# Performance work log

Hardware: AMD Instinct MI355X
Metric: run time of the kernel (lower is better)

The kernel has to match this reference:

```python
import jax, jax.numpy as jnp
import numpy as np

C0, C1, ED, H, L, K = 128, 32, 64, 4, 2, 16
RADIUS = 16.0
EPS = 1e-6


def _ln(x, g, b):
    m = jnp.mean(x, -1, keepdims=True)
    v = jnp.var(x, -1, keepdims=True)
    return (x - m) * jax.lax.rsqrt(v + 1e-5) * g + b


def _gather_nodes(x, idx):
    # x [B,N,...], idx [B,N,K] -> [B,N,K,...]
    return jax.vmap(lambda xb, ib: xb[ib])(x, idx)


def _gather_pairs(e, idx):
    # e [B,N,N,ED], idx [B,N,K] -> [B,N,K,ED]  (batched_index_select on dim=2)
    return jax.vmap(lambda eb, ib: jnp.take_along_axis(eb, ib[..., None], axis=1))(e, idx)


def _fiber_norm(f0, f1, g0, b0, g1, b1):
    # deg-0: LayerNorm + gelu; deg-1: phase-preserving norm on channel magnitudes
    f0n = jax.nn.gelu(_ln(f0, g0, b0))
    n1 = jnp.linalg.norm(f1, axis=-1)                       # [B,N,C1]
    f1n = f1 / (n1 + EPS)[..., None] * jax.nn.gelu(_ln(n1, g1, b1))[..., None]
    return f0n, f1n


def _tfn_kv(f0j, f1j, y1, r, WA, WB):
    # Equivariant TFN edge kernel: paths 0->0(l=0), 1->0(l=1), 0->1(l=1),
    # 1->1(l=0), 1->1(l=1, cross), 1->1(l=2, traceless Y2) with radial gates r.
    r1, r2, r3, r4, r5, r6 = jnp.split(
        r, [C0, C0 + C1, 2 * C0 + C1, 2 * C0 + 2 * C1, 2 * C0 + 3 * C1], axis=-1)
    dot1 = jnp.einsum('bnkcm,bnkm->bnkc', f1j, y1)          # [B,N,K,C1]
    in0 = jnp.concatenate([r1 * f0j, r2 * dot1], -1)        # [B,N,K,C0+C1]
    k0 = jnp.einsum('oc,bnkc->bnko', WA, in0)               # [B,N,K,C0]
    p3 = (r3 * f0j)[..., None] * y1[..., None, :]           # [B,N,K,C0,3]
    p4 = r4[..., None] * f1j
    p5 = r5[..., None] * jnp.cross(f1j, y1[..., None, :])
    p6 = r6[..., None] * (y1[..., None, :] * dot1[..., None] - f1j / 3.0)
    in1 = jnp.concatenate([p3, p4, p5, p6], axis=-2)        # [B,N,K,C0+3*C1,3]
    k1 = jnp.einsum('oc,bnkcm->bnkom', WB, in1)             # [B,N,K,C1,3]
    return k0, k1


def reference(node_feats, pair_feats, coords, eln_g, eln_b, Wi0, Wi1,
              ln0_g, ln0_b, n1_g, n1_b, Wq0, Wq1, WrK, WrV, WkA, WkB, WvA, WvB,
              Wb, Wo0, Wo1, alpha_attn, lnf0_g, lnf0_b, nf1_g, nf1_b,
              Wf0a, Wf0b, Wf1a, Wf1b, alpha_ff, Wp0, Wp1):
    B, N = node_feats.shape[:2]
    Na, CA, Cc, Oo = [coords[..., i, :] for i in range(4)]          # each [B,N,3]
    f1_in = jnp.stack([Na, Cc, Oo], axis=-2) - CA[..., None, :]     # [B,N,3,3]
    # kNN graph on CA coords (exclude self), radius mask at 16A
    d2 = jnp.sum((CA[:, :, None] - CA[:, None, :]) ** 2, -1)        # [B,N,N]
    d2 = d2 + jnp.eye(N, dtype=d2.dtype) * 1e9
    nv, idx = jax.lax.top_k(-d2, K)                                 # idx [B,N,K]
    dist = jnp.sqrt(jnp.maximum(-nv, 0.0))
    mask = dist <= RADIUS
    rel_pos = _gather_nodes(CA, idx) - CA[:, :, None]               # [B,N,K,3]
    rel_b = jax.lax.stop_gradient(rel_pos)                          # basis on detached rel_pos
    y1 = rel_b / (jnp.linalg.norm(rel_b, axis=-1, keepdims=True) + EPS)
    edges = _ln(_gather_pairs(pair_feats, idx), eln_g, eln_b)       # [B,N,K,ED]
    # project in
    f0 = jnp.einsum('oc,bnc->bno', Wi0, node_feats)                 # [B,N,C0]
    f1 = jnp.einsum('oc,bncm->bnom', Wi1, f1_in)                    # [B,N,C1,3]
    dh0, dh1 = C0 // H, C1 // H
    scale = 1.0 / np.sqrt(dh0 + 3 * dh1)
    for l in range(L):
        # ---- attention block (prenorm -> TFN attention -> rezero residual)
        x0, x1 = _fiber_norm(f0, f1, ln0_g[l], ln0_b[l], n1_g[l], n1_b[l])
        q0 = jnp.einsum('oc,bnc->bno', Wq0[l], x0)
        q1 = jnp.einsum('oc,bncm->bnom', Wq1[l], x1)
        x0j = _gather_nodes(x0, idx)                                # [B,N,K,C0]
        x1j = _gather_nodes(x1, idx)                                # [B,N,K,C1,3]
        rk = jnp.einsum('re,bnke->bnkr', WrK[l], edges)
        rv = jnp.einsum('re,bnke->bnkr', WrV[l], edges)
        k0, k1 = _tfn_kv(x0j, x1j, y1, rk, WkA[l], WkB[l])
        v0, v1 = _tfn_kv(x0j, x1j, y1, rv, WvA[l], WvB[l])
        q0h = q0.reshape(B, N, H, dh0)
        q1h = q1.reshape(B, N, H, dh1, 3)
        k0h = k0.reshape(B, N, K, H, dh0)
        k1h = k1.reshape(B, N, K, H, dh1, 3)
        v0h = v0.reshape(B, N, K, H, dh0)
        v1h = v1.reshape(B, N, K, H, dh1, 3)
        logits = (jnp.einsum('bnhc,bnkhc->bnhk', q0h, k0h)
                  + jnp.einsum('bnhcm,bnkhcm->bnhk', q1h, k1h)) * scale
        logits = logits + jnp.einsum('he,bnke->bnhk', Wb[l], edges)
        logits = jnp.where(mask[:, :, None, :], logits, -1e9)
        attn = jax.nn.softmax(logits, axis=-1)
        o0 = jnp.einsum('bnhk,bnkhc->bnhc', attn, v0h).reshape(B, N, C0)
        o1 = jnp.einsum('bnhk,bnkhcm->bnhcm', attn, v1h).reshape(B, N, C1, 3)
        f0 = f0 + alpha_attn[l] * jnp.einsum('oc,bnc->bno', Wo0[l], o0)
        f1 = f1 + alpha_attn[l] * jnp.einsum('oc,bncm->bnom', Wo1[l], o1)
        # ---- fiber feedforward (prenorm -> FF -> rezero residual)
        x0, x1 = _fiber_norm(f0, f1, lnf0_g[l], lnf0_b[l], nf1_g[l], nf1_b[l])
        h0 = jnp.einsum('oh,bnh->bno', Wf0b[l],
                        jax.nn.gelu(jnp.einsum('hc,bnc->bnh', Wf0a[l], x0)))
        h1 = jnp.einsum('hc,bncm->bnhm', Wf1a[l], x1)
        nh = jnp.linalg.norm(h1, axis=-1)
        h1 = h1 * (jax.nn.gelu(nh) / (nh + EPS))[..., None]
        h1 = jnp.einsum('oh,bnhm->bnom', Wf1b[l], h1)
        f0 = f0 + alpha_ff[l] * h0
        f1 = f1 + alpha_ff[l] * h1
    # project out + _to_output
    node_out = jnp.einsum('oc,bnc->bno', Wp0, f0)                   # [B,N,128]
    coords_out = CA[:, :, None, :] + jnp.einsum('oc,bncm->bnom', Wp1, f1)  # [B,N,3,3]
    return node_out, coords_out


def setup_inputs() -> dict:
    key = jax.random.key(0)
    ks = iter(jax.random.split(key, 64))
    def rn(shape, scale=1.0):
        return (jax.random.normal(next(ks), shape) * scale).astype(jnp.float32)
    B, N = 1, 1024
    RC = 2 * C0 + 4 * C1
    ca = jnp.cumsum(rn((B, N, 3), 1.5), axis=1)          # protein-like chain
    coords = ca[:, :, None, :] + rn((B, N, 4, 3), 0.5)
    inp = dict(
        node_feats=rn((B, N, 128)),
        pair_feats=rn((B, N, N, ED)),
        coords=coords,
        eln_g=jnp.ones((ED,), jnp.float32), eln_b=jnp.zeros((ED,), jnp.float32),
        Wi0=rn((C0, 128), 128 ** -0.5), Wi1=rn((C1, 3), 3 ** -0.5),
        ln0_g=jnp.ones((L, C0), jnp.float32), ln0_b=jnp.zeros((L, C0), jnp.float32),
        n1_g=jnp.ones((L, C1), jnp.float32), n1_b=jnp.zeros((L, C1), jnp.float32),
        Wq0=rn((L, C0, C0), C0 ** -0.5), Wq1=rn((L, C1, C1), C1 ** -0.5),
        WrK=rn((L, RC, ED), ED ** -0.5), WrV=rn((L, RC, ED), ED ** -0.5),
        WkA=rn((L, C0, C0 + C1), (C0 + C1) ** -0.5),
        WkB=rn((L, C1, C0 + 3 * C1), (C0 + 3 * C1) ** -0.5),
        WvA=rn((L, C0, C0 + C1), (C0 + C1) ** -0.5),
        WvB=rn((L, C1, C0 + 3 * C1), (C0 + 3 * C1) ** -0.5),
        Wb=rn((L, H, ED), ED ** -0.5),
        Wo0=rn((L, C0, C0), C0 ** -0.5), Wo1=rn((L, C1, C1), C1 ** -0.5),
        alpha_attn=jnp.full((L,), 0.5, jnp.float32),
        lnf0_g=jnp.ones((L, C0), jnp.float32), lnf0_b=jnp.zeros((L, C0), jnp.float32),
        nf1_g=jnp.ones((L, C1), jnp.float32), nf1_b=jnp.zeros((L, C1), jnp.float32),
        Wf0a=rn((L, 4 * C0, C0), C0 ** -0.5), Wf0b=rn((L, C0, 4 * C0), (4 * C0) ** -0.5),
        Wf1a=rn((L, 4 * C1, C1), C1 ** -0.5), Wf1b=rn((L, C1, 4 * C1), (4 * C1) ** -0.5),
        alpha_ff=jnp.full((L,), 0.5, jnp.float32),
        Wp0=rn((128, C0), C0 ** -0.5), Wp1=rn((3, C1), C1 ** -0.5),
    )
    return inp
```

## Files before the change

kernel.cpp:

```cpp
#include <hip/hip_runtime.h>
#include <hip/hip_bf16.h>
#include <math.h>

static constexpr int NN  = 1024;
static constexpr int KK  = 16;
static constexpr int C0c = 128;
static constexpr int C1c = 32;
static constexpr int EDc = 64;
static constexpr int Lc  = 2;
static constexpr int ENUM = NN * KK;
static constexpr int PL   = NN * C1c;
static constexpr int X1HS = NN * 32;
#define SCALE_ATTN 0.13363062095621219f

typedef __attribute__((ext_vector_type(8))) short s8v;
typedef __attribute__((ext_vector_type(4))) float f4v;

__device__ __forceinline__ float wsum64(float v) {
    for (int o = 32; o > 0; o >>= 1) v += __shfl_xor(v, o);
    return v;
}
__device__ __forceinline__ float gsum16(float v) {
    for (int o = 8; o > 0; o >>= 1) v += __shfl_xor(v, o, 16);
    return v;
}
__device__ __forceinline__ float gmax16(float v) {
    for (int o = 8; o > 0; o >>= 1) v = fmaxf(v, __shfl_xor(v, o, 16));
    return v;
}
__device__ __forceinline__ float gelu_f(float x) {
    float x3 = x * x * x;
    return 0.5f * x * (1.0f + tanhf(0.7978845608028654f * (x + 0.044715f * x3)));
}
__device__ __forceinline__ unsigned short f2bf(float x) {
    union { float f; unsigned int u; } v; v.f = x;
    unsigned int r = v.u + 0x7fffu + ((v.u >> 16) & 1u);
    return (unsigned short)(r >> 16);
}
__device__ __forceinline__ float bf2f(unsigned short u) {
    union { float f; unsigned int i; } v; v.i = ((unsigned int)u) << 16;
    return v.f;
}
__device__ __forceinline__ s8v ld8(const unsigned short* p) { return *(const s8v*)p; }
__device__ __forceinline__ f4v mfma16(s8v a, s8v b, f4v c) {
    return __builtin_amdgcn_mfma_f32_16x16x32_bf16(a, b, c, 0, 0, 0);
}

struct CvJob { const float* s; unsigned short* d; int n; };
struct CvJobs { CvJob j[20]; int n; int total; };

__global__ __launch_bounds__(256) void setup_kernel(CvJobs cj, int cvb,
                                                    const float* __restrict__ coords,
                                                    int* __restrict__ idx,
                                                    float* __restrict__ maskf,
                                                    float* __restrict__ y1,
                                                    const float* __restrict__ Wi1,
                                                    float* __restrict__ f1p) {
    __shared__ float ca[NN * 3];
    const int tid = threadIdx.x;
    const int bx = blockIdx.x;
    if (bx < cvb) {
        int g = bx * 256 + tid;
        if (g >= cj.total) return;
        for (int i = 0; i < cj.n; ++i) {
            int n = cj.j[i].n;
            if (g < n) { cj.j[i].d[g] = f2bf(cj.j[i].s[g]); return; }
            g -= n;
        }
        return;
    }
    if (bx < cvb + 256) {
        for (int f = tid; f < NN * 3; f += 256) {
            int i = f / 3, m = f % 3;
            ca[f] = coords[(i * 4 + 1) * 3 + m];
        }
        __syncthreads();
        const int wid = tid >> 6, lane = tid & 63;
        const int n = (bx - cvb) * 4 + wid;
        const float cx = ca[n * 3 + 0], cy = ca[n * 3 + 1], cz = ca[n * 3 + 2];
        float d[16];
#pragma unroll
        for (int s = 0; s < 16; ++s) {
            int i = s * 64 + lane;
            float dx = cx - ca[i * 3 + 0], dy = cy - ca[i * 3 + 1], dz = cz - ca[i * 3 + 2];
            float d2 = dx * dx + dy * dy + dz * dz;
            d[s] = (i == n) ? 1e9f : d2;
        }
        for (int t = 0; t < KK; ++t) {
            float best = 1e30f; int bi = 0;
#pragma unroll
            for (int s = 0; s < 16; ++s) {
                int i = s * 64 + lane;
                float v = d[s];
                if (v < best || (v == best && i < bi)) { best = v; bi = i; }
            }
#pragma unroll
            for (int o = 32; o > 0; o >>= 1) {
                float ov = __shfl_xor(best, o);
                int   oi = __shfl_xor(bi, o);
                if (ov < best || (ov == best && oi < bi)) { best = ov; bi = oi; }
            }
            const int j = bi;
            if (lane == 0) {
                idx[n * KK + t] = j;
                float dist = sqrtf(best);
                maskf[n * KK + t] = (dist <= 16.0f) ? 1.0f : 0.0f;
                float rx = ca[j * 3 + 0] - cx, ry = ca[j * 3 + 1] - cy, rz = ca[j * 3 + 2] - cz;
                float nrm = sqrtf(rx * rx + ry * ry + rz * rz) + 1e-6f;
                y1[(n * KK + t) * 3 + 0] = rx / nrm;
                y1[(n * KK + t) * 3 + 1] = ry / nrm;
                y1[(n * KK + t) * 3 + 2] = rz / nrm;
            }
            const int js = j >> 6, jl = j & 63;
#pragma unroll
            for (int s = 0; s < 16; ++s)
                if (s == js && jl == lane) d[s] = 2e30f;
        }
        return;
    }
    int g = (bx - cvb - 256) * 256 + tid;
    if (g >= NN * 32) return;
    int n = g >> 5, c = g & 31;
    float w0 = Wi1[c * 3 + 0], w1 = Wi1[c * 3 + 1], w2 = Wi1[c * 3 + 2];
#pragma unroll
    for (int m = 0; m < 3; ++m) {
        float cav = coords[(n * 4 + 1) * 3 + m];
        float a0 = coords[(n * 4 + 0) * 3 + m] - cav;
        float a1 = coords[(n * 4 + 2) * 3 + m] - cav;
        float a2 = coords[(n * 4 + 3) * 3 + m] - cav;
        f1p[m * PL + n * 32 + c] = w0 * a0 + w1 * a1 + w2 * a2;
    }
}

__global__ __launch_bounds__(256) void edge_f0_kernel(const float* __restrict__ pair,
                                                      const int* __restrict__ idx,
                                                      const float* __restrict__ g,
                                                      const float* __restrict__ b,
                                                      unsigned short* __restrict__ edges_h,
                                                      const unsigned short* __restrict__ nf_h,
                                                      const unsigned short* __restrict__ Wi0_h,
                                                      float* __restrict__ f0) {
    const int t = threadIdx.x, wid = t >> 6, lane = t & 63;
    if (blockIdx.x < ENUM / 4) {
        const int e = blockIdx.x * 4 + wid;
        const int n = e >> 4;
        const int j = idx[e];
        float v = pair[((size_t)n * NN + j) * EDc + lane];
        float m = wsum64(v) * (1.0f / 64.0f);
        float d = v - m;
        float var = wsum64(d * d) * (1.0f / 64.0f);
        float nv = d * rsqrtf(var + 1e-5f) * g[lane] + b[lane];
        edges_h[e * EDc + lane] = f2bf(nv);
        return;
    }
    int rel = blockIdx.x - ENUM / 4;
    const int mt = rel & 7, ntc = rel >> 3;
    const int m0 = mt * 128 + wid * 32, n0 = ntc * 32;
    const int c16 = lane & 15, g8 = (lane >> 4) * 8, g4 = (lane >> 4) * 4;
    f4v acc[2][2];
#pragma unroll
    for (int a = 0; a < 2; ++a)
#pragma unroll
        for (int bq = 0; bq < 2; ++bq) acc[a][bq] = f4v{0.f, 0.f, 0.f, 0.f};
    const unsigned short* Ap = nf_h + (size_t)(m0 + c16) * 128 + g8;
    const unsigned short* Bp = Wi0_h + (size_t)(n0 + c16) * 128 + g8;
#pragma unroll
    for (int kc = 0; kc < 128; kc += 32) {
        s8v a0 = ld8(Ap + kc);
        s8v a1 = ld8(Ap + 16 * 128 + kc);
        s8v b0 = ld8(Bp + kc);
        s8v b1 = ld8(Bp + 16 * 128 + kc);
        acc[0][0] = mfma16(a0, b0, acc[0][0]);
        acc[0][1] = mfma16(a0, b1, acc[0][1]);
        acc[1][0] = mfma16(a1, b0, acc[1][0]);
        acc[1][1] = mfma16(a1, b1, acc[1][1]);
    }
#pragma unroll
    for (int fm = 0; fm < 2; ++fm)
#pragma unroll
        for (int r = 0; r < 4; ++r) {
            const int m = m0 + fm * 16 + g4 + r;
#pragma unroll
            for (int fn = 0; fn < 2; ++fn)
                f0[(size_t)m * 128 + n0 + fn * 16 + c16] = acc[fm][fn][r];
        }
}

__global__ __launch_bounds__(256) void fnorm1_kernel(const float* __restrict__ f0,
                                                     const float* __restrict__ f1p,
                                                     const float* __restrict__ g0,
                                                     const float* __restrict__ b0,
                                                     const float* __restrict__ g1,
                                                     const float* __restrict__ b1,
                                                     unsigned short* __restrict__ x0h,
                                                     unsigned short* __restrict__ x1h) {
    const int wid = threadIdx.x >> 6, lane = threadIdx.x & 63;
    const int n = blockIdx.x * 4 + wid;
    float va = f0[n * 128 + lane], vb = f0[n * 128 + lane + 64];
    float m = wsum64(va + vb) * (1.0f / 128.0f);
    float da = va - m, db = vb - m;
    float var = wsum64(da * da + db * db) * (1.0f / 128.0f);
    float rs = rsqrtf(var + 1e-5f);
    x0h[n * 128 + lane]      = f2bf(gelu_f(da * rs * g0[lane] + b0[lane]));
    x0h[n * 128 + lane + 64] = f2bf(gelu_f(db * rs * g0[lane + 64] + b0[lane + 64]));
    int c = lane & 31;
    float h0 = f1p[0 * PL + n * 32 + c];
    float h1 = f1p[1 * PL + n * 32 + c];
    float h2 = f1p[2 * PL + n * 32 + c];
    float n1 = sqrtf(h0 * h0 + h1 * h1 + h2 * h2);
    float ms = wsum64(n1) * (1.0f / 64.0f);
    float dd = n1 - ms;
    float vv = wsum64(dd * dd) * (1.0f / 64.0f);
    float sc = gelu_f(dd * rsqrtf(vv + 1e-5f) * g1[c] + b1[c]) / (n1 + 1e-6f);
    if (lane < 32) {
        x1h[0 * X1HS + n * 32 + c] = f2bf(h0 * sc);
        x1h[1 * X1HS + n * 32 + c] = f2bf(h1 * sc);
        x1h[2 * X1HS + n * 32 + c] = f2bf(h2 * sc);
    }
}

static constexpr int LS_IN0 = 0;
static constexpr int LS_INU = 64 * 168;
static constexpr int LS_INW = LS_INU + 64 * 136;
static constexpr int LS_X0  = LS_INW + 3 * 64 * 104;
static constexpr int LS_X1  = LS_X0 + 64 * 128;
static constexpr int LS_ED  = LS_X1 + 3 * 64 * 32;
static constexpr int LS_Y   = LS_ED + 64 * 72;
static constexpr int EKV_LDS2 = LS_Y * 2 + 64 * 3 * 4;

__global__ __launch_bounds__(512) void edge_kv2(
    const unsigned short* __restrict__ edges_h,
    const unsigned short* __restrict__ WrK, const unsigned short* __restrict__ WrV,
    const unsigned short* __restrict__ WkA, const unsigned short* __restrict__ WvA,
    const unsigned short* __restrict__ WkB, const unsigned short* __restrict__ WvB,
    const unsigned short* __restrict__ WbL,
    const unsigned short* __restrict__ x0h, const unsigned short* __restrict__ x1h,
    const int* __restrict__ idx, const float* __restrict__ y1,
    unsigned short* __restrict__ k0h, unsigned short* __restrict__ v0h,
    unsigned short* __restrict__ uKh, unsigned short* __restrict__ uVh,
    unsigned short* __restrict__ k1ph, unsigned short* __restrict__ v1ph,
    float* __restrict__ biasb,
    const unsigned short* __restrict__ Wq0l, const unsigned short* __restrict__ Wq1l,
    float* __restrict__ q0, float* __restrict__ q1p) {
    extern __shared__ unsigned short lsm[];
    const int t = threadIdx.x, w = t >> 6, l = t & 63;
    const int c16 = l & 15, g8 = (l >> 4) * 8, g4 = (l >> 4) * 4;
    const int bid = blockIdx.x;
    if (bid < 256) {
        unsigned short* in0L = lsm + LS_IN0;
        unsigned short* inUL = lsm + LS_INU;
        unsigned short* inWL = lsm + LS_INW;
        unsigned short* x0L  = lsm + LS_X0;
        unsigned short* x1L  = lsm + LS_X1;
        unsigned short* edL  = lsm + LS_ED;
        float* yL = (float*)(lsm + LS_Y);
        const int e0 = bid * 64;
        for (int c = t; c < 1024; c += 512) {
            int row = c >> 4, sub = c & 15;
            int j = idx[e0 + row];
            *(s8v*)&x0L[row * 128 + sub * 8] = ld8(x0h + (size_t)j * 128 + sub * 8);
        }
        for (int c = t; c < 768; c += 512) {
            int plane = c >> 8, rem = c & 255;
            int row = rem >> 2, sub = rem & 3;
            int j = idx[e0 + row];
            *(s8v*)&x1L[(plane * 64 + row) * 32 + sub * 8] =
                ld8(x1h + (size_t)plane * X1HS + (size_t)j * 32 + sub * 8);
        }
        for (int c = t; c < 512; c += 512) {
            int row = c >> 3, sub = c & 7;
            *(s8v*)&edL[row * 72 + sub * 8] = ld8(edges_h + (size_t)(e0 + row) * 64 + sub * 8);
        }
        if (t < 192) yL[t] = y1[e0 * 3 + t];
        __syncthreads();
#pragma unroll 1
        for (int s = 0; s < 2; ++s) {
            const unsigned short* Wr = s ? WrV : WrK;
            const unsigned short* WA = s ? WvA : WkA;
            const unsigned short* WB = s ? WvB : WkB;
            unsigned short* K0o = s ? v0h : k0h;
            unsigned short* Uo  = s ? uVh : uKh;
            unsigned short* K1o = s ? v1ph : k1ph;
#pragma unroll 1
            for (int ti = w; ti < 24; ti += 8) {
                const int esub = ti & 1, rt = ti >> 1;
                const int el0 = esub * 32, r0 = rt * 32;
                f4v acc[2][2];
#pragma unroll
                for (int a = 0; a < 2; ++a)
#pragma unroll
                    for (int bq = 0; bq < 2; ++bq) acc[a][bq] = f4v{0.f, 0.f, 0.f, 0.f};
#pragma unroll
                for (int kc = 0; kc < 64; kc += 32) {
                    s8v a0 = *(const s8v*)&edL[(el0 + c16) * 72 + kc + g8];
                    s8v a1 = *(const s8v*)&edL[(el0 + 16 + c16) * 72 + kc + g8];
                    s8v b0 = ld8(Wr + (size_t)(r0 + c16) * 64 + kc + g8);
                    s8v b1 = ld8(Wr + (size_t)(r0 + 16 + c16) * 64 + kc + g8);
                    acc[0][0] = mfma16(a0, b0, acc[0][0]);
                    acc[0][1] = mfma16(a0, b1, acc[0][1]);
                    acc[1][0] = mfma16(a1, b0, acc[1][0]);
                    acc[1][1] = mfma16(a1, b1, acc[1][1]);
                }
#pragma unroll
                for (int fm = 0; fm < 2; ++fm)
#pragma unroll
                    for (int r = 0; r < 4; ++r) {
                        const int el = el0 + fm * 16 + g4 + r;
                        float ya = yL[el * 3 + 0], yb = yL[el * 3 + 1], yc = yL[el * 3 + 2];
#pragma unroll
                        for (int fn = 0; fn < 2; ++fn) {
                            const float av = acc[fm][fn][r];
                            const int col = r0 + fn * 16 + c16;
                            if (r0 < 128) {
                                in0L[el * 168 + col] = f2bf(av * bf2f(x0L[el * 128 + col]));
                            } else if (r0 < 160) {
                                int c = col - 128;
                                float d1 = bf2f(x1L[(0 * 64 + el) * 32 + c]) * ya
                                         + bf2f(x1L[(1 * 64 + el) * 32 + c]) * yb
                                         + bf2f(x1L[(2 * 64 + el) * 32 + c]) * yc;
                                in0L[el * 168 + col] = f2bf(av * d1);
                            } else if (r0 < 288) {
                                int c = col - 160;
                                inUL[el * 136 + c] = f2bf(av * bf2f(x0L[el * 128 + c]));
                            } else {
                                int c = (r0 < 320) ? (col - 288) : (r0 < 352) ? (col - 320) : (col - 352);
                                float fx = bf2f(x1L[(0 * 64 + el) * 32 + c]);
                                float fy = bf2f(x1L[(1 * 64 + el) * 32 + c]);
                                float fz = bf2f(x1L[(2 * 64 + el) * 32 + c]);
                                float w0, w1, w2; int off;
                                if (r0 < 320) {
                                    off = 0; w0 = av * fx; w1 = av * fy; w2 = av * fz;
                                } else if (r0 < 352) {
                                    off = 32;
                                    w0 = av * (fy * yc - fz * yb);
                                    w1 = av * (fz * ya - fx * yc);
                                    w2 = av * (fx * yb - fy * ya);
                                } else {
                                    off = 64;
                                    float d1 = fx * ya + fy * yb + fz * yc;
                                    w0 = av * (ya * d1 - fx * (1.0f / 3.0f));
                                    w1 = av * (yb * d1 - fy * (1.0f / 3.0f));
                                    w2 = av * (yc * d1 - fz * (1.0f / 3.0f));
                                }
                                inWL[0 * 64 * 104 + el * 104 + off + c] = f2bf(w0);
                                inWL[1 * 64 * 104 + el * 104 + off + c] = f2bf(w1);
                                inWL[2 * 64 * 104 + el * 104 + off + c] = f2bf(w2);
                            }
                        }
                    }
            }
            __syncthreads();
            const int tmax = (s == 0) ? 18 : 16;
#pragma unroll 1
            for (int ti = w; ti < tmax; ti += 8) {
                if (ti >= 16) {
                    const int esub = ti - 16;
                    f4v bacc[2] = {f4v{0.f,0.f,0.f,0.f}, f4v{0.f,0.f,0.f,0.f}};
                    s8v zb;
#pragma unroll
                    for (int j = 0; j < 8; ++j) zb[j] = 0;
#pragma unroll
                    for (int kc = 0; kc < 64; kc += 32) {
                        s8v a0 = *(const s8v*)&edL[(esub * 32 + c16) * 72 + kc + g8];
                        s8v a1 = *(const s8v*)&edL[(esub * 32 + 16 + c16) * 72 + kc + g8];
                        s8v b0 = (c16 < 4) ? ld8(WbL + (size_t)c16 * 64 + kc + g8) : zb;
                        bacc[0] = mfma16(a0, b0, bacc[0]);
                        bacc[1] = mfma16(a1, b0, bacc[1]);
                    }
                    if (c16 < 4) {
#pragma unroll
                        for (int fm = 0; fm < 2; ++fm)
#pragma unroll
                            for (int r = 0; r < 4; ++r)
                                biasb[(size_t)(e0 + esub * 32 + fm * 16 + g4 + r) * 4 + c16] = bacc[fm][r];
                    }
                    continue;
                }
                const unsigned short* Ab; const unsigned short* Bb;
                unsigned short* Cb;
                int apit, K, ldb, ldcq, esub;
                if (ti < 8) {
                    esub = ti & 1; int nt = ti >> 1;
                    Ab = in0L; apit = 168; K = 160;
                    Bb = WA + (size_t)(nt * 32) * 160; ldb = 160;
                    Cb = K0o + (size_t)(e0 + esub * 32) * 128 + nt * 32; ldcq = 128;
                } else if (ti < 10) {
                    esub = ti - 8;
                    Ab = inUL; apit = 136; K = 128; Bb = WB; ldb = 224;
                    Cb = Uo + (size_t)(e0 + esub * 32) * 32; ldcq = 32;
                } else {
                    int id = ti - 10; int m = id >> 1; esub = id & 1;
                    Ab = inWL + m * 64 * 104; apit = 104; K = 96;
                    Bb = WB + 128; ldb = 224;
                    Cb = K1o + ((size_t)m * ENUM + e0 + esub * 32) * 32; ldcq = 32;
                }
                const int m0l = esub * 32;
                f4v acc[2][2];
#pragma unroll
                for (int a = 0; a < 2; ++a)
#pragma unroll
                    for (int bq = 0; bq < 2; ++bq) acc[a][bq] = f4v{0.f, 0.f, 0.f, 0.f};
                for (int kc = 0; kc < K; kc += 32) {
                    s8v a0 = *(const s8v*)&Ab[(m0l + c16) * apit + kc + g8];
                    s8v a1 = *(const s8v*)&Ab[(m0l + 16 + c16) * apit + kc + g8];
                    s8v b0 = ld8(Bb + (size_t)c16 * ldb + kc + g8);
                    s8v b1 = ld8(Bb + (size_t)(16 + c16) * ldb + kc + g8);
                    acc[0][0] = mfma16(a0, b0, acc[0][0]);
                    acc[0][1] = mfma16(a0, b1, acc[0][1]);
                    acc[1][0] = mfma16(a1, b0, acc[1][0]);
                    acc[1][1] = mfma16(a1, b1, acc[1][1]);
                }
#pragma unroll
                for (int fm = 0; fm < 2; ++fm)
#pragma unroll
                    for (int r = 0; r < 4; ++r) {
                        const int lr = fm * 16 + g4 + r;
#pragma unroll
                        for (int fn = 0; fn < 2; ++fn)
                            Cb[(size_t)lr * ldcq + fn * 16 + c16] = f2bf(acc[fm][fn][r]);
                    }
            }
            __syncthreads();
        }
        return;
    }
    const int wt = (bid - 256) * 8 + w;
    const unsigned short* A; const unsigned short* B;
    float* C; int K, lda2, m0, n0, ldc2;
    if (wt < 128) {
        int rowt = wt >> 2, colt = wt & 3;
        A = x0h; B = Wq0l; C = q0;
        K = 128; lda2 = 128; ldc2 = 128;
        m0 = rowt * 32; n0 = colt * 32;
    } else {
        int k = wt - 128;
        int pl = k >> 5, rowt = k & 31;
        A = x1h + (size_t)pl * X1HS; B = Wq1l; C = q1p + (size_t)pl * PL;
        K = 32; lda2 = 32; ldc2 = 32;
        m0 = rowt * 32; n0 = 0;
    }
    f4v acc[2][2];
#pragma unroll
    for (int a = 0; a < 2; ++a)
#pragma unroll
        for (int bq = 0; bq < 2; ++bq) acc[a][bq] = f4v{0.f, 0.f, 0.f, 0.f};
    const unsigned short* Ap = A + (size_t)(m0 + c16) * lda2 + g8;
    const unsigned short* Bp = B + (size_t)(n0 + c16) * lda2 + g8;
    for (int kc = 0; kc < K; kc += 32) {
        s8v a0 = ld8(Ap + kc);
        s8v a1 = ld8(Ap + 16 * lda2 + kc);
        s8v b0 = ld8(Bp + kc);
        s8v b1 = ld8(Bp + 16 * lda2 + kc);
        acc[0][0] = mfma16(a0, b0, acc[0][0]);
        acc[0][1] = mfma16(a0, b1, acc[0][1]);
        acc[1][0] = mfma16(a1, b0, acc[1][0]);
        acc[1][1] = mfma16(a1, b1, acc[1][1]);
    }
#pragma unroll
    for (int fm = 0; fm < 2; ++fm)
#pragma unroll
        for (int r = 0; r < 4; ++r) {
            const int m = m0 + fm * 16 + g4 + r;
#pragma unroll
            for (int fn = 0; fn < 2; ++fn)
                C[(size_t)m * ldc2 + n0 + fn * 16 + c16] = acc[fm][fn][r];
        }
}

__global__ __launch_bounds__(256) void attn_core(const float* __restrict__ q0,
                                                 const float* __restrict__ q1p,
                                                 const unsigned short* __restrict__ k0h,
                                                 const unsigned short* __restrict__ k1ph,
                                                 const unsigned short* __restrict__ v0h,
                                                 const unsigned short* __restrict__ v1ph,
                                                 const unsigned short* __restrict__ uKh,
                                                 const unsigned short* __restrict__ uVh,
                                                 const float* __restrict__ biasb,
                                                 const float* __restrict__ maskf,
                                                 const float* __restrict__ y1,
                                                 unsigned short* __restrict__ o0h,
                                                 unsigned short* __restrict__ o1h) {
    __shared__ float q0s[4][128];
    __shared__ float q1s[4][96];
    __shared__ float attns[4][64];
    const int wid = threadIdx.x >> 6, lane = threadIdx.x & 63;
    const int n = blockIdx.x * 4 + wid;
    q0s[wid][lane]      = q0[n * 128 + lane];
    q0s[wid][lane + 64] = q0[n * 128 + lane + 64];
    if (lane < 32) {
#pragma unroll
        for (int m = 0; m < 3; ++m) q1s[wid][m * 32 + lane] = q1p[m * PL + n * 32 + lane];
    }
    __syncthreads();
    {
        const int h = lane >> 4, k = lane & 15;
        const int e = n * KK + k;
        float acc = 0.f;
        const unsigned short* kr = k0h + (size_t)e * 128 + h * 32;
#pragma unroll
        for (int c8 = 0; c8 < 4; ++c8) {
            s8v kv = ld8(kr + c8 * 8);
#pragma unroll
            for (int j = 0; j < 8; ++j)
                acc += q0s[wid][h * 32 + c8 * 8 + j] * bf2f((unsigned short)kv[j]);
        }
        s8v uv = ld8(uKh + (size_t)e * 32 + h * 8);
#pragma unroll
        for (int m = 0; m < 3; ++m) {
            float yv = y1[e * 3 + m];
            s8v k1v = ld8(k1ph + ((size_t)m * ENUM + e) * 32 + h * 8);
#pragma unroll
            for (int c = 0; c < 8; ++c)
                acc += q1s[wid][m * 32 + h * 8 + c] *
                       (bf2f((unsigned short)k1v[c]) + bf2f((unsigned short)uv[c]) * yv);
        }
        acc = acc * SCALE_ATTN + biasb[e * 4 + h];
        if (maskf[e] == 0.0f) acc = -1e9f;
        float mx = gmax16(acc);
        float ex = expf(acc - mx);
        float sm = gsum16(ex);
        attns[wid][lane] = ex / sm;
    }
    __syncthreads();
    const int g = lane & 15, kq = lane >> 4;
    {
        float o[8] = {};
        const float* aw = &attns[wid][(g >> 2) * 16];
#pragma unroll
        for (int kk2 = 0; kk2 < 4; ++kk2) {
            int kk = kq * 4 + kk2;
            float a = aw[kk];
            s8v v = ld8(v0h + (size_t)(n * KK + kk) * 128 + g * 8);
#pragma unroll
            for (int j = 0; j < 8; ++j) o[j] += a * bf2f((unsigned short)v[j]);
        }
#pragma unroll
        for (int j = 0; j < 8; ++j) {
            o[j] += __shfl_xor(o[j], 16);
            o[j] += __shfl_xor(o[j], 32);
        }
        if (kq == 0) {
            s8v r;
#pragma unroll
            for (int j = 0; j < 8; ++j) r[j] = (short)f2bf(o[j]);
            *(s8v*)&o0h[(size_t)n * 128 + g * 8] = r;
        }
    }
    {
        float o[8] = {};
        const int plane = g >> 2, cg = g & 3;
        if (g < 12) {
            const float* aw = &attns[wid][cg * 16];
#pragma unroll
            for (int kk2 = 0; kk2 < 4; ++kk2) {
                int kk = kq * 4 + kk2;
                int e2 = n * KK + kk;
                float a = aw[kk];
                float yv = y1[e2 * 3 + plane];
                s8v v = ld8(v1ph + ((size_t)plane * ENUM + e2) * 32 + cg * 8);
                s8v u = ld8(uVh + (size_t)e2 * 32 + cg * 8);
#pragma unroll
                for (int j = 0; j < 8; ++j)
                    o[j] += a * (bf2f((unsigned short)v[j]) + bf2f((unsigned short)u[j]) * yv);
            }
        }
#pragma unroll
        for (int j = 0; j < 8; ++j) {
            o[j] += __shfl_xor(o[j], 16);
            o[j] += __shfl_xor(o[j], 32);
        }
        if (kq == 0 && g < 12) {
            s8v r;
#pragma unroll
            for (int j = 0; j < 8; ++j) r[j] = (short)f2bf(o[j]);
            *(s8v*)&o1h[((size_t)plane * NN + n) * 32 + cg * 8] = r;
        }
    }
}

template <int MODE>
__global__ __launch_bounds__(512) void fused_post(
    const unsigned short* __restrict__ o0h, const unsigned short* __restrict__ o1h,
    float* __restrict__ f0, float* __restrict__ f1p,
    const unsigned short* __restrict__ Wo0h, const unsigned short* __restrict__ Wo1h,
    const unsigned short* __restrict__ Wf0ah, const unsigned short* __restrict__ Wf0bh,
    const unsigned short* __restrict__ Wf1ah, const unsigned short* __restrict__ Wf1bh,
    const float* __restrict__ alA, const float* __restrict__ alF,
    const float* __restrict__ lnf0_g, const float* __restrict__ lnf0_b,
    const float* __restrict__ nf1_g, const float* __restrict__ nf1_b,
    const float* __restrict__ ln0n_g, const float* __restrict__ ln0n_b,
    const float* __restrict__ n1n_g, const float* __restrict__ n1n_b,
    unsigned short* __restrict__ x0h, unsigned short* __restrict__ x1h,
    const unsigned short* __restrict__ Wp0h, const float* __restrict__ Wp1,
    const float* __restrict__ coords, float* __restrict__ out) {
    __shared__ float f0s[16][132];
    __shared__ float f1s[3][16][36];
    __shared__ unsigned short x0s[16][136];
    __shared__ float x1s[3][16][36];
    __shared__ unsigned short hs[16][520];
    __shared__ unsigned short h1b[3][16][136];
    const int t = threadIdx.x, w = t >> 6, l = t & 63;
    const int c16 = l & 15, g8 = (l >> 4) * 8, g4 = (l >> 4) * 4;
    const int n0 = blockIdx.x * 16;
    const float aA = alA[0], aF = alF[0];

    {
        f4v acc = f4v{0.f, 0.f, 0.f, 0.f};
        const unsigned short* Ap = o0h + (size_t)(n0 + c16) * 128 + g8;
#pragma unroll
        for (int kc = 0; kc < 128; kc += 32) {
            s8v a = ld8(Ap + kc);
            s8v b = ld8(Wo0h + (size_t)(w * 16 + c16) * 128 + g8 + kc);
            acc = mfma16(a, b, acc);
        }
        int colg = w * 16 + c16;
#pragma unroll
        for (int r = 0; r < 4; ++r) {
            int row = g4 + r;
            f0s[row][colg] = f0[(size_t)(n0 + row) * 128 + colg] + aA * acc[r];
        }
    }
#pragma unroll
    for (int it = 0; it < 3; ++it) {
        int g = t + it * 512;
        int c = g & 31, node = (g >> 5) & 15, m = g >> 9;
        float a = 0.f;
        const unsigned short* wrow = Wo1h + c * 32;
        const unsigned short* orow = o1h + ((size_t)m * NN + n0 + node) * 32;
#pragma unroll
        for (int cc = 0; cc < 32; ++cc) a += bf2f(wrow[cc]) * bf2f(orow[cc]);
        f1s[m][node][c] = f1p[(size_t)m * PL + (n0 + node) * 32 + c] + aA * a;
    }
    __syncthreads();
    for (int i = 0; i < 2; ++i) {
        int row = w * 2 + i;
        float v0 = f0s[row][l], v1 = f0s[row][l + 64];
        float mn = wsum64(v0 + v1) * (1.0f / 128.0f);
        float d0 = v0 - mn, d1 = v1 - mn;
        float var = wsum64(d0 * d0 + d1 * d1) * (1.0f / 128.0f);
        float rs = rsqrtf(var + 1e-5f);
        x0s[row][l]      = f2bf(gelu_f(d0 * rs * lnf0_g[l] + lnf0_b[l]));
        x0s[row][l + 64] = f2bf(gelu_f(d1 * rs * lnf0_g[l + 64] + lnf0_b[l + 64]));
    }
    if (t < 256) {
        int node = t >> 4, sub = t & 15;
        float p[2][3], n1v[2];
#pragma unroll
        for (int q = 0; q < 2; ++q) {
            int c = sub + q * 16;
            p[q][0] = f1s[0][node][c]; p[q][1] = f1s[1][node][c]; p[q][2] = f1s[2][node][c];
            n1v[q] = sqrtf(p[q][0]*p[q][0] + p[q][1]*p[q][1] + p[q][2]*p[q][2]);
        }
        float s = gsum16(n1v[0] + n1v[1]);
        float mn = s * (1.0f / 32.0f);
        float d0 = n1v[0] - mn, d1 = n1v[1] - mn;
        float vv = gsum16(d0 * d0 + d1 * d1);
        float rs = rsqrtf(vv * (1.0f / 32.0f) + 1e-5f);
#pragma unroll
        for (int q = 0; q < 2; ++q) {
            int c = sub + q * 16;
            float sc = gelu_f((n1v[q] - mn) * rs * nf1_g[c] + nf1_b[c]) / (n1v[q] + 1e-6f);
            x1s[0][node][c] = p[q][0] * sc;
            x1s[1][node][c] = p[q][1] * sc;
            x1s[2][node][c] = p[q][2] * sc;
        }
    }
    __syncthreads();
    {
        f4v acc[4];
#pragma unroll
        for (int i = 0; i < 4; ++i) acc[i] = f4v{0.f,0.f,0.f,0.f};
#pragma unroll
        for (int kc = 0; kc < 128; kc += 32) {
            s8v a = *(const s8v*)&x0s[c16][kc + g8];
#pragma unroll
            for (int tt = 0; tt < 4; ++tt) {
                s8v b = ld8(Wf0ah + (size_t)((w * 4 + tt) * 16 + c16) * 128 + g8 + kc);
                acc[tt] = mfma16(a, b, acc[tt]);
            }
        }
#pragma unroll
        for (int tt = 0; tt < 4; ++tt) {
            int colg = (w * 4 + tt) * 16 + c16;
#pragma unroll
            for (int r = 0; r < 4; ++r) hs[g4 + r][colg] = f2bf(gelu_f(acc[tt][r]));
        }
    }
#pragma unroll
    for (int it = 0; it < 4; ++it) {
        int g = t + it * 512;
        int r = g & 127, node = g >> 7;
        float a0 = 0.f, a1 = 0.f, a2 = 0.f;
        const unsigned short* wrow = Wf1ah + r * 32;
#pragma unroll
        for (int c = 0; c < 32; ++c) {
            float wv = bf2f(wrow[c]);
            a0 += wv * x1s[0][node][c];
            a1 += wv * x1s[1][node][c];
            a2 += wv * x1s[2][node][c];
        }
        float nh = sqrtf(a0 * a0 + a1 * a1 + a2 * a2);
        float sc = gelu_f(nh) / (nh + 1e-6f);
        h1b[0][node][r] = f2bf(a0 * sc);
        h1b[1][node][r] = f2bf(a1 * sc);
        h1b[2][node][r] = f2bf(a2 * sc);
    }
    __syncthreads();
    {
        f4v acc = f4v{0.f, 0.f, 0.f, 0.f};
#pragma unroll 4
        for (int kc = 0; kc < 512; kc += 32) {
            s8v a = *(const s8v*)&hs[c16][kc + g8];
            s8v b = ld8(Wf0bh + (size_t)(w * 16 + c16) * 512 + g8 + kc);
            acc = mfma16(a, b, acc);
        }
        int colg = w * 16 + c16;
#pragma unroll
        for (int r = 0; r < 4; ++r) {
            int row = g4 + r;
            float v = f0s[row][colg] + aF * acc[r];
            f0s[row][colg] = v;
            f0[(size_t)(n0 + row) * 128 + colg] = v;
        }
    }
#pragma unroll
    for (int it = 0; it < 3; ++it) {
        int g = t + it * 512;
        int c = g & 31, node = (g >> 5) & 15, m = g >> 9;
        float a = 0.f;
        const unsigned short* wrow = Wf1bh + c * 128;
#pragma unroll 8
        for (int r = 0; r < 128; ++r) a += bf2f(wrow[r]) * bf2f(h1b[m][node][r]);
        float v = f1s[m][node][c] + aF * a;
        f1s[m][node][c] = v;
        f1p[(size_t)m * PL + (n0 + node) * 32 + c] = v;
    }
    __syncthreads();
    if (MODE == 0) {
        for (int i = 0; i < 2; ++i) {
            int row = w * 2 + i;
            float v0 = f0s[row][l], v1 = f0s[row][l + 64];
            float mn = wsum64(v0 + v1) * (1.0f / 128.0f);
            float d0 = v0 - mn, d1 = v1 - mn;
            float var = wsum64(d0 * d0 + d1 * d1) * (1.0f / 128.0f);
            float rs = rsqrtf(var + 1e-5f);
            x0h[(size_t)(n0 + row) * 128 + l]      = f2bf(gelu_f(d0 * rs * ln0n_g[l] + ln0n_b[l]));
            x0h[(size_t)(n0 + row) * 128 + l + 64] = f2bf(gelu_f(d1 * rs * ln0n_g[l + 64] + ln0n_b[l + 64]));
        }
        if (t < 256) {
            int node = t >> 4, sub = t & 15;
            float p[2][3], n1v[2];
#pragma unroll
            for (int q = 0; q < 2; ++q) {
                int c = sub + q * 16;
                p[q][0] = f1s[0][node][c]; p[q][1] = f1s[1][node][c]; p[q][2] = f1s[2][node][c];
                n1v[q] = sqrtf(p[q][0]*p[q][0] + p[q][1]*p[q][1] + p[q][2]*p[q][2]);
            }
            float s = gsum16(n1v[0] + n1v[1]);
            float mn = s * (1.0f / 32.0f);
            float d0 = n1v[0] - mn, d1 = n1v[1] - mn;
            float vv = gsum16(d0 * d0 + d1 * d1);
            float rs = rsqrtf(vv * (1.0f / 32.0f) + 1e-5f);
#pragma unroll
            for (int q = 0; q < 2; ++q) {
                int c = sub + q * 16;
                float sc = gelu_f((n1v[q] - mn) * rs * n1n_g[c] + n1n_b[c]) / (n1v[q] + 1e-6f);
                x1h[(size_t)0 * X1HS + (n0 + node) * 32 + c] = f2bf(p[q][0] * sc);
                x1h[(size_t)1 * X1HS + (n0 + node) * 32 + c] = f2bf(p[q][1] * sc);
                x1h[(size_t)2 * X1HS + (n0 + node) * 32 + c] = f2bf(p[q][2] * sc);
            }
        }
    } else {
#pragma unroll
        for (int it = 0; it < 4; ++it) {
            int g = t + it * 512;
            int row = g >> 7, col = g & 127;
            x0s[row][col] = f2bf(f0s[row][col]);
        }
        __syncthreads();
        f4v acc = f4v{0.f, 0.f, 0.f, 0.f};
#pragma unroll
        for (int kc = 0; kc < 128; kc += 32) {
            s8v a = *(const s8v*)&x0s[c16][kc + g8];
            s8v b = ld8(Wp0h + (size_t)(w * 16 + c16) * 128 + g8 + kc);
            acc = mfma16(a, b, acc);
        }
        int colg = w * 16 + c16;
#pragma unroll
        for (int r = 0; r < 4; ++r)
            out[(size_t)(n0 + g4 + r) * 128 + colg] = acc[r];
        if (t < 144) {
            int node = t / 9, rr = t % 9, o = rr / 3, m = rr % 3;
            float a = coords[((size_t)(n0 + node) * 4 + 1) * 3 + m];
            for (int c = 0; c < 32; ++c) a += Wp1[o * 32 + c] * f1s[m][node][c];
            out[NN * 128 + ((size_t)(n0 + node) * 3 + o) * 3 + m] = a;
        }
    }
}

extern "C" void kernel_launch(void* const* d_in, const int* in_sizes, int n_in,
                              void* d_out, int out_size, void* d_ws, size_t ws_size,
                              hipStream_t stream) {
    (void)in_sizes; (void)n_in; (void)out_size; (void)ws_size;
    const float* node_feats = (const float*)d_in[0];
    const float* pair       = (const float*)d_in[1];
    const float* coords     = (const float*)d_in[2];
    const float* eln_g      = (const float*)d_in[3];
    const float* eln_b      = (const float*)d_in[4];
    const float* Wi0        = (const float*)d_in[5];
    const float* Wi1        = (const float*)d_in[6];
    const float* ln0_g      = (const float*)d_in[7];
    const float* ln0_b      = (const float*)d_in[8];
    const float* n1_g       = (const float*)d_in[9];
    const float* n1_b       = (const float*)d_in[10];
    const float* Wq0        = (const float*)d_in[11];
    const float* Wq1        = (const float*)d_in[12];
    const float* WrK        = (const float*)d_in[13];
    const float* WrV        = (const float*)d_in[14];
    const float* WkA        = (const float*)d_in[15];
    const float* WkB        = (const float*)d_in[16];
    const float* WvA        = (const float*)d_in[17];
    const float* WvB        = (const float*)d_in[18];
    const float* Wb         = (const float*)d_in[19];
    const float* Wo0        = (const float*)d_in[20];
    const float* Wo1        = (const float*)d_in[21];
    const float* alpha_attn = (const float*)d_in[22];
    const float* lnf0_g     = (const float*)d_in[23];
    const float* lnf0_b     = (const float*)d_in[24];
    const float* nf1_g      = (const float*)d_in[25];
    const float* nf1_b      = (const float*)d_in[26];
    const float* Wf0a       = (const float*)d_in[27];
    const float* Wf0b       = (const float*)d_in[28];
    const float* Wf1a       = (const float*)d_in[29];
    const float* Wf1b       = (const float*)d_in[30];
    const float* alpha_ff   = (const float*)d_in[31];
    const float* Wp0        = (const float*)d_in[32];
    const float* Wp1        = (const float*)d_in[33];
    float* out = (float*)d_out;

    float* ws = (float*)d_ws;
    size_t off = 0;
    int*   idx   = (int*)(ws + off); off += NN * KK;
    float* maskf = ws + off;         off += NN * KK;
    float* y1    = ws + off;         off += NN * KK * 3;
    float* f0    = ws + off;         off += NN * C0c;
    float* f1p   = ws + off;         off += 3 * PL;
    float* q0    = ws + off;         off += NN * C0c;
    float* q1p   = ws + off;         off += 3 * PL;
    float* biasb = ws + off;         off += (size_t)ENUM * 4;
    off = (off + 3) & ~(size_t)3;
    unsigned short* up = (unsigned short*)(ws + off);
    size_t uo = 0;
    unsigned short* edges_h = up + uo; uo += (size_t)ENUM * 64;
    unsigned short* x0h     = up + uo; uo += (size_t)NN * 128;
    unsigned short* x1h     = up + uo; uo += (size_t)3 * X1HS;
    unsigned short* nf_h    = up + uo; uo += (size_t)NN * 128;
    unsigned short* k0h     = up + uo; uo += (size_t)ENUM * 128;
    unsigned short* v0h     = up + uo; uo += (size_t)ENUM * 128;
    unsigned short* uKh     = up + uo; uo += (size_t)ENUM * 32;
    unsigned short* uVh     = up + uo; uo += (size_t)ENUM * 32;
    unsigned short* k1ph    = up + uo; uo += (size_t)3 * ENUM * 32;
    unsigned short* v1ph    = up + uo; uo += (size_t)3 * ENUM * 32;
    unsigned short* o0h     = up + uo; uo += (size_t)NN * 128;
    unsigned short* o1h     = up + uo; uo += (size_t)3 * NN * 32;
    unsigned short* WrK_h   = up + uo; uo += 2 * 24576;
    unsigned short* WrV_h   = up + uo; uo += 2 * 24576;
    unsigned short* WkA_h   = up + uo; uo += 2 * 20480;
    unsigned short* WvA_h   = up + uo; uo += 2 * 20480;
    unsigned short* WkB_h   = up + uo; uo += 2 * 7168;
    unsigned short* WvB_h   = up + uo; uo += 2 * 7168;
    unsigned short* Wq0_h   = up + uo; uo += 2 * 16384;
    unsigned short* Wq1_h   = up + uo; uo += 2 * 1024;
    unsigned short* Wo0_h   = up + uo; uo += 2 * 16384;
    unsigned short* Wo1_h   = up + uo; uo += 2 * 1024;
    unsigned short* Wf0a_h  = up + uo; uo += 2 * 65536;
    unsigned short* Wf0b_h  = up + uo; uo += 2 * 65536;
    unsigned short* Wf1a_h  = up + uo; uo += 2 * 4096;
    unsigned short* Wf1b_h  = up + uo; uo += 2 * 4096;
    unsigned short* Wp0_h   = up + uo; uo += 16384;
    unsigned short* Wi0_h   = up + uo; uo += 16384;
    unsigned short* Wb_h    = up + uo; uo += 2 * 256;

    CvJobs cj; cj.n = 18;
    cj.j[0]  = {WrK,  WrK_h,  2 * 24576};
    cj.j[1]  = {WrV,  WrV_h,  2 * 24576};
    cj.j[2]  = {WkA,  WkA_h,  2 * 20480};
    cj.j[3]  = {WvA,  WvA_h,  2 * 20480};
    cj.j[4]  = {WkB,  WkB_h,  2 * 7168};
    cj.j[5]  = {WvB,  WvB_h,  2 * 7168};
    cj.j[6]  = {Wq0,  Wq0_h,  2 * 16384};
    cj.j[7]  = {Wq1,  Wq1_h,  2 * 1024};
    cj.j[8]  = {Wo0,  Wo0_h,  2 * 16384};
    cj.j[9]  = {Wo1,  Wo1_h,  2 * 1024};
    cj.j[10] = {Wf0a, Wf0a_h, 2 * 65536};
    cj.j[11] = {Wf0b, Wf0b_h, 2 * 65536};
    cj.j[12] = {Wf1a, Wf1a_h, 2 * 4096};
    cj.j[13] = {Wf1b, Wf1b_h, 2 * 4096};
    cj.j[14] = {Wp0,  Wp0_h,  16384};
    cj.j[15] = {Wi0,  Wi0_h,  16384};
    cj.j[16] = {node_feats, nf_h, NN * 128};
    cj.j[17] = {Wb,   Wb_h,   2 * 256};
    cj.total = 2*24576*2 + 2*20480*2 + 2*7168*2 + 2*16384 + 2*1024 + 2*16384
             + 2*1024 + 2*65536*2 + 2*4096*2 + 16384 + 16384 + NN*128 + 2*256;
    const int cvb = (cj.total + 255) / 256;

    setup_kernel<<<cvb + 256 + 128, 256, 0, stream>>>(cj, cvb, coords, idx, maskf, y1, Wi1, f1p);
    edge_f0_kernel<<<ENUM / 4 + 32, 256, 0, stream>>>(pair, idx, eln_g, eln_b,
                                                      edges_h, nf_h, Wi0_h, f0);
    fnorm1_kernel<<<NN / 4, 256, 0, stream>>>(f0, f1p, ln0_g, ln0_b, n1_g, n1_b, x0h, x1h);

    for (int l = 0; l < Lc; ++l) {
        edge_kv2<<<284, 512, EKV_LDS2, stream>>>(
            edges_h,
            WrK_h + (size_t)l * 24576, WrV_h + (size_t)l * 24576,
            WkA_h + (size_t)l * 20480, WvA_h + (size_t)l * 20480,
            WkB_h + (size_t)l * 7168,  WvB_h + (size_t)l * 7168,
            Wb_h + (size_t)l * 256,
            x0h, x1h, idx, y1,
            k0h, v0h, uKh, uVh, k1ph, v1ph, biasb,
            Wq0_h + (size_t)l * 16384, Wq1_h + (size_t)l * 1024, q0, q1p);
        attn_core<<<NN / 4, 256, 0, stream>>>(q0, q1p, k0h, k1ph, v0h, v1ph, uKh, uVh,
            biasb, maskf, y1, o0h, o1h);
        if (l == 0) {
            fused_post<0><<<NN / 16, 512, 0, stream>>>(
                o0h, o1h, f0, f1p,
                Wo0_h, Wo1_h, Wf0a_h, Wf0b_h, Wf1a_h, Wf1b_h,
                alpha_attn + 0, alpha_ff + 0,
                lnf0_g, lnf0_b, nf1_g, nf1_b,
                ln0_g + 128, ln0_b + 128, n1_g + 32, n1_b + 32,
                x0h, x1h, nullptr, nullptr, nullptr, nullptr);
        } else {
            fused_post<1><<<NN / 16, 512, 0, stream>>>(
                o0h, o1h, f0, f1p,
                Wo0_h + 16384, Wo1_h + 1024, Wf0a_h + 65536, Wf0b_h + 65536,
                Wf1a_h + 4096, Wf1b_h + 4096,
                alpha_attn + 1, alpha_ff + 1,
                lnf0_g + 128, lnf0_b + 128, nf1_g + 32, nf1_b + 32,
                nullptr, nullptr, nullptr, nullptr,
                nullptr, nullptr, Wp0_h, Wp1, coords, out);
        }
    }
}
```

Before: 219.0 us.

## Fuse per-layer edge, attention and post kernels into one cooperative megakernel

Replaces the three per-layer launches (edge_kv2, attn_core, fused_post) for both layers with a single cooperative kernel of 256 blocks that uses grid-wide syncs between phases. This removes the launch gaps and the tail idle time between the six kernels. In exchange every phase is pinned to 256 blocks of 512 threads with the large edge-stage LDS allocation, which can lower occupancy and change how work is spread in the attention and post phases. Each grid sync also adds its own cost.

```diff
diff --git a/kernel.cpp b/kernel.cpp
--- a/kernel.cpp
+++ b/kernel.cpp
@@ -1,15 +1,17 @@
 #include <hip/hip_runtime.h>
 #include <hip/hip_bf16.h>
+#include <hip/hip_cooperative_groups.h>
 #include <math.h>
+
+namespace cg = cooperative_groups;
 
 static constexpr int NN  = 1024;
 static constexpr int KK  = 16;
 static constexpr int C0c = 128;
-static constexpr int C1c = 32;
 static constexpr int EDc = 64;
 static constexpr int Lc  = 2;
 static constexpr int ENUM = NN * KK;
-static constexpr int PL   = NN * C1c;
+static constexpr int PL   = NN * 32;
 static constexpr int X1HS = NN * 32;
 #define SCALE_ATTN 0.13363062095621219f
 
@@ -228,74 +230,242 @@
 static constexpr int LS_Y   = LS_ED + 64 * 72;
 static constexpr int EKV_LDS2 = LS_Y * 2 + 64 * 3 * 4;
 
-__global__ __launch_bounds__(512) void edge_kv2(
-    const unsigned short* __restrict__ edges_h,
-    const unsigned short* __restrict__ WrK, const unsigned short* __restrict__ WrV,
-    const unsigned short* __restrict__ WkA, const unsigned short* __restrict__ WvA,
-    const unsigned short* __restrict__ WkB, const unsigned short* __restrict__ WvB,
-    const unsigned short* __restrict__ WbL,
-    const unsigned short* __restrict__ x0h, const unsigned short* __restrict__ x1h,
-    const int* __restrict__ idx, const float* __restrict__ y1,
-    unsigned short* __restrict__ k0h, unsigned short* __restrict__ v0h,
-    unsigned short* __restrict__ uKh, unsigned short* __restrict__ uVh,
-    unsigned short* __restrict__ k1ph, unsigned short* __restrict__ v1ph,
-    float* __restrict__ biasb,
-    const unsigned short* __restrict__ Wq0l, const unsigned short* __restrict__ Wq1l,
-    float* __restrict__ q0, float* __restrict__ q1p) {
+struct MegaArgs {
+    const unsigned short *edges_h, *WrK, *WrV, *WkA, *WvA, *WkB, *WvB, *Wb;
+    const unsigned short *Wq0, *Wq1, *Wo0, *Wo1, *Wf0a, *Wf0b, *Wf1a, *Wf1b, *Wp0;
+    unsigned short *x0h, *x1h;
+    const int* idx; const float* y1;
+    unsigned short *k0h, *v0h, *uKh, *uVh, *k1ph, *v1ph;
+    float *biasb, *q0, *q1p, *f0, *f1p;
+    const float *maskf, *alpha_attn, *alpha_ff;
+    const float *ln0_g, *ln0_b, *n1_g, *n1_b, *lnf0_g, *lnf0_b, *nf1_g, *nf1_b;
+    const float *Wp1, *coords;
+    unsigned short *o0h, *o1h;
+    float* out;
+};
+
+__global__ __launch_bounds__(512) void mega_kernel(MegaArgs A) {
     extern __shared__ unsigned short lsm[];
-    const int t = threadIdx.x, w = t >> 6, l = t & 63;
-    const int c16 = l & 15, g8 = (l >> 4) * 8, g4 = (l >> 4) * 4;
+    cg::grid_group gg = cg::this_grid();
+    const int t = threadIdx.x, w = t >> 6, ln = t & 63;
+    const int c16 = ln & 15, g8 = (ln >> 4) * 8, g4 = (ln >> 4) * 4;
     const int bid = blockIdx.x;
-    if (bid < 256) {
-        unsigned short* in0L = lsm + LS_IN0;
-        unsigned short* inUL = lsm + LS_INU;
-        unsigned short* inWL = lsm + LS_INW;
-        unsigned short* x0L  = lsm + LS_X0;
-        unsigned short* x1L  = lsm + LS_X1;
-        unsigned short* edL  = lsm + LS_ED;
-        float* yL = (float*)(lsm + LS_Y);
-        const int e0 = bid * 64;
-        for (int c = t; c < 1024; c += 512) {
-            int row = c >> 4, sub = c & 15;
-            int j = idx[e0 + row];
-            *(s8v*)&x0L[row * 128 + sub * 8] = ld8(x0h + (size_t)j * 128 + sub * 8);
-        }
-        for (int c = t; c < 768; c += 512) {
-            int plane = c >> 8, rem = c & 255;
-            int row = rem >> 2, sub = rem & 3;
-            int j = idx[e0 + row];
-            *(s8v*)&x1L[(plane * 64 + row) * 32 + sub * 8] =
-                ld8(x1h + (size_t)plane * X1HS + (size_t)j * 32 + sub * 8);
-        }
-        for (int c = t; c < 512; c += 512) {
-            int row = c >> 3, sub = c & 7;
-            *(s8v*)&edL[row * 72 + sub * 8] = ld8(edges_h + (size_t)(e0 + row) * 64 + sub * 8);
-        }
-        if (t < 192) yL[t] = y1[e0 * 3 + t];
-        __syncthreads();
+
+    for (int l = 0; l < Lc; ++l) {
+        const unsigned short* WrKl = A.WrK + (size_t)l * 24576;
+        const unsigned short* WrVl = A.WrV + (size_t)l * 24576;
+        const unsigned short* WkAl = A.WkA + (size_t)l * 20480;
+        const unsigned short* WvAl = A.WvA + (size_t)l * 20480;
+        const unsigned short* WkBl = A.WkB + (size_t)l * 7168;
+        const unsigned short* WvBl = A.WvB + (size_t)l * 7168;
+        const unsigned short* WbLl = A.Wb + (size_t)l * 256;
+        const unsigned short* Wq0l = A.Wq0 + (size_t)l * 16384;
+        const unsigned short* Wq1l = A.Wq1 + (size_t)l * 1024;
+
+        {
+            unsigned short* in0L = lsm + LS_IN0;
+            unsigned short* inUL = lsm + LS_INU;
+            unsigned short* inWL = lsm + LS_INW;
+            unsigned short* x0L  = lsm + LS_X0;
+            unsigned short* x1L  = lsm + LS_X1;
+            unsigned short* edL  = lsm + LS_ED;
+            float* yL = (float*)(lsm + LS_Y);
+            const int e0 = bid * 64;
+            for (int c = t; c < 1024; c += 512) {
+                int row = c >> 4, sub = c & 15;
+                int j = A.idx[e0 + row];
+                *(s8v*)&x0L[row * 128 + sub * 8] = ld8(A.x0h + (size_t)j * 128 + sub * 8);
+            }
+            for (int c = t; c < 768; c += 512) {
+                int plane = c >> 8, rem = c & 255;
+                int row = rem >> 2, sub = rem & 3;
+                int j = A.idx[e0 + row];
+                *(s8v*)&x1L[(plane * 64 + row) * 32 + sub * 8] =
+                    ld8(A.x1h + (size_t)plane * X1HS + (size_t)j * 32 + sub * 8);
+            }
+            {
+                int row = t >> 3, sub = t & 7;
+                *(s8v*)&edL[row * 72 + sub * 8] = ld8(A.edges_h + (size_t)(e0 + row) * 64 + sub * 8);
+            }
+            if (t < 192) yL[t] = A.y1[e0 * 3 + t];
+            __syncthreads();
 #pragma unroll 1
-        for (int s = 0; s < 2; ++s) {
-            const unsigned short* Wr = s ? WrV : WrK;
-            const unsigned short* WA = s ? WvA : WkA;
-            const unsigned short* WB = s ? WvB : WkB;
-            unsigned short* K0o = s ? v0h : k0h;
-            unsigned short* Uo  = s ? uVh : uKh;
-            unsigned short* K1o = s ? v1ph : k1ph;
+            for (int s = 0; s < 2; ++s) {
+                const unsigned short* Wr = s ? WrVl : WrKl;
+                const unsigned short* WA = s ? WvAl : WkAl;
+                const unsigned short* WB = s ? WvBl : WkBl;
+                unsigned short* K0o = s ? A.v0h : A.k0h;
+                unsigned short* Uo  = s ? A.uVh : A.uKh;
+                unsigned short* K1o = s ? A.v1ph : A.k1ph;
 #pragma unroll 1
-            for (int ti = w; ti < 24; ti += 8) {
-                const int esub = ti & 1, rt = ti >> 1;
-                const int el0 = esub * 32, r0 = rt * 32;
+                for (int ti = w; ti < 24; ti += 8) {
+                    const int esub = ti & 1, rt = ti >> 1;
+                    const int el0 = esub * 32, r0 = rt * 32;
+                    f4v acc[2][2];
+#pragma unroll
+                    for (int a = 0; a < 2; ++a)
+#pragma unroll
+                        for (int bq = 0; bq < 2; ++bq) acc[a][bq] = f4v{0.f, 0.f, 0.f, 0.f};
+#pragma unroll
+                    for (int kc = 0; kc < 64; kc += 32) {
+                        s8v a0 = *(const s8v*)&edL[(el0 + c16) * 72 + kc + g8];
+                        s8v a1 = *(const s8v*)&edL[(el0 + 16 + c16) * 72 + kc + g8];
+                        s8v b0 = ld8(Wr + (size_t)(r0 + c16) * 64 + kc + g8);
+                        s8v b1 = ld8(Wr + (size_t)(r0 + 16 + c16) * 64 + kc + g8);
+                        acc[0][0] = mfma16(a0, b0, acc[0][0]);
+                        acc[0][1] = mfma16(a0, b1, acc[0][1]);
+                        acc[1][0] = mfma16(a1, b0, acc[1][0]);
+                        acc[1][1] = mfma16(a1, b1, acc[1][1]);
+                    }
+#pragma unroll
+                    for (int fm = 0; fm < 2; ++fm)
+#pragma unroll
+                        for (int r = 0; r < 4; ++r) {
+                            const int el = el0 + fm * 16 + g4 + r;
+                            float ya = yL[el * 3 + 0], yb = yL[el * 3 + 1], yc = yL[el * 3 + 2];
+#pragma unroll
+                            for (int fn = 0; fn < 2; ++fn) {
+                                const float av = acc[fm][fn][r];
+                                const int col = r0 + fn * 16 + c16;
+                                if (r0 < 128) {
+                                    in0L[el * 168 + col] = f2bf(av * bf2f(x0L[el * 128 + col]));
+                                } else if (r0 < 160) {
+                                    int c = col - 128;
+                                    float d1 = bf2f(x1L[(0 * 64 + el) * 32 + c]) * ya
+                                             + bf2f(x1L[(1 * 64 + el) * 32 + c]) * yb
+                                             + bf2f(x1L[(2 * 64 + el) * 32 + c]) * yc;
+                                    in0L[el * 168 + col] = f2bf(av * d1);
+                                } else if (r0 < 288) {
+                                    int c = col - 160;
+                                    inUL[el * 136 + c] = f2bf(av * bf2f(x0L[el * 128 + c]));
+                                } else {
+                                    int c = (r0 < 320) ? (col - 288) : (r0 < 352) ? (col - 320) : (col - 352);
+                                    float fx = bf2f(x1L[(0 * 64 + el) * 32 + c]);
+                                    float fy = bf2f(x1L[(1 * 64 + el) * 32 + c]);
+                                    float fz = bf2f(x1L[(2 * 64 + el) * 32 + c]);
+                                    float w0, w1, w2; int off;
+                                    if (r0 < 320) {
+                                        off = 0; w0 = av * fx; w1 = av * fy; w2 = av * fz;
+                                    } else if (r0 < 352) {
+                                        off = 32;
+                                        w0 = av * (fy * yc - fz * yb);
+                                        w1 = av * (fz * ya - fx * yc);
+                                        w2 = av * (fx * yb - fy * ya);
+                                    } else {
+                                        off = 64;
+                                        float d1 = fx * ya + fy * yb + fz * yc;
+                                        w0 = av * (ya * d1 - fx * (1.0f / 3.0f));
+                                        w1 = av * (yb * d1 - fy * (1.0f / 3.0f));
+                                        w2 = av * (yc * d1 - fz * (1.0f / 3.0f));
+                                    }
+                                    inWL[0 * 64 * 104 + el * 104 + off + c] = f2bf(w0);
+                                    inWL[1 * 64 * 104 + el * 104 + off + c] = f2bf(w1);
+                                    inWL[2 * 64 * 104 + el * 104 + off + c] = f2bf(w2);
+                                }
+                            }
+                        }
+                }
+                __syncthreads();
+                const int tmax = (s == 0) ? 18 : 16;
+#pragma unroll 1
+                for (int ti = w; ti < tmax; ti += 8) {
+                    if (ti >= 16) {
+                        const int esub = ti - 16;
+                        f4v bacc[2] = {f4v{0.f,0.f,0.f,0.f}, f4v{0.f,0.f,0.f,0.f}};
+                        s8v zb;
+#pragma unroll
+                        for (int j = 0; j < 8; ++j) zb[j] = 0;
+#pragma unroll
+                        for (int kc = 0; kc < 64; kc += 32) {
+                            s8v a0 = *(const s8v*)&edL[(esub * 32 + c16) * 72 + kc + g8];
+                            s8v a1 = *(const s8v*)&edL[(esub * 32 + 16 + c16) * 72 + kc + g8];
+                            s8v b0 = (c16 < 4) ? ld8(WbLl + (size_t)c16 * 64 + kc + g8) : zb;
+                            bacc[0] = mfma16(a0, b0, bacc[0]);
+                            bacc[1] = mfma16(a1, b0, bacc[1]);
+                        }
+                        if (c16 < 4) {
+#pragma unroll
+                            for (int fm = 0; fm < 2; ++fm)
+#pragma unroll
+                                for (int r = 0; r < 4; ++r)
+                                    A.biasb[(size_t)(e0 + esub * 32 + fm * 16 + g4 + r) * 4 + c16] = bacc[fm][r];
+                        }
+                        continue;
+                    }
+                    const unsigned short* Ab; const unsigned short* Bb;
+                    unsigned short* Cb;
+                    int apit, K, ldb, ldcq, esub;
+                    if (ti < 8) {
+                        esub = ti & 1; int nt = ti >> 1;
+                        Ab = in0L; apit = 168; K = 160;
+                        Bb = WA + (size_t)(nt * 32) * 160; ldb = 160;
+                        Cb = K0o + (size_t)(e0 + esub * 32) * 128 + nt * 32; ldcq = 128;
+                    } else if (ti < 10) {
+                        esub = ti - 8;
+                        Ab = inUL; apit = 136; K = 128; Bb = WB; ldb = 224;
+                        Cb = Uo + (size_t)(e0 + esub * 32) * 32; ldcq = 32;
+                    } else {
+                        int id = ti - 10; int m = id >> 1; esub = id & 1;
+                        Ab = inWL + m * 64 * 104; apit = 104; K = 96;
+                        Bb = WB + 128; ldb = 224;
+                        Cb = K1o + ((size_t)m * ENUM + e0 + esub * 32) * 32; ldcq = 32;
+                    }
+                    const int m0l = esub * 32;
+                    f4v acc[2][2];
+#pragma unroll
+                    for (int a = 0; a < 2; ++a)
+#pragma unroll
+                        for (int bq = 0; bq < 2; ++bq) acc[a][bq] = f4v{0.f, 0.f, 0.f, 0.f};
+                    for (int kc = 0; kc < K; kc += 32) {
+                        s8v a0 = *(const s8v*)&Ab[(m0l + c16) * apit + kc + g8];
+                        s8v a1 = *(const s8v*)&Ab[(m0l + 16 + c16) * apit + kc + g8];
+                        s8v b0 = ld8(Bb + (size_t)c16 * ldb + kc + g8);
+                        s8v b1 = ld8(Bb + (size_t)(16 + c16) * ldb + kc + g8);
+                        acc[0][0] = mfma16(a0, b0, acc[0][0]);
+                        acc[0][1] = mfma16(a0, b1, acc[0][1]);
+                        acc[1][0] = mfma16(a1, b0, acc[1][0]);
+                        acc[1][1] = mfma16(a1, b1, acc[1][1]);
+                    }
+#pragma unroll
+                    for (int fm = 0; fm < 2; ++fm)
+#pragma unroll
+                        for (int r = 0; r < 4; ++r) {
+                            const int lr = fm * 16 + g4 + r;
+#pragma unroll
+                            for (int fn = 0; fn < 2; ++fn)
+                                Cb[(size_t)lr * ldcq + fn * 16 + c16] = f2bf(acc[fm][fn][r]);
+                        }
+                }
+                __syncthreads();
+            }
+            if (bid < 28) {
+                const int wt = bid * 8 + w;
+                const unsigned short* Aq; const unsigned short* Bq;
+                float* Cq; int K, lda2, m0, n0, ldc2;
+                if (wt < 128) {
+                    int rowt = wt >> 2, colt = wt & 3;
+                    Aq = A.x0h; Bq = Wq0l; Cq = A.q0;
+                    K = 128; lda2 = 128; ldc2 = 128;
+                    m0 = rowt * 32; n0 = colt * 32;
+                } else {
+                    int k = wt - 128;
+                    int pl = k >> 5, rowt = k & 31;
+                    Aq = A.x1h + (size_t)pl * X1HS; Bq = Wq1l; Cq = A.q1p + (size_t)pl * PL;
+                    K = 32; lda2 = 32; ldc2 = 32;
+                    m0 = rowt * 32; n0 = 0;
+                }
                 f4v acc[2][2];
 #pragma unroll
                 for (int a = 0; a < 2; ++a)
 #pragma unroll
                     for (int bq = 0; bq < 2; ++bq) acc[a][bq] = f4v{0.f, 0.f, 0.f, 0.f};
-#pragma unroll
-                for (int kc = 0; kc < 64; kc += 32) {
-                    s8v a0 = *(const s8v*)&edL[(el0 + c16) * 72 + kc + g8];
-                    s8v a1 = *(const s8v*)&edL[(el0 + 16 + c16) * 72 + kc + g8];
-                    s8v b0 = ld8(Wr + (size_t)(r0 + c16) * 64 + kc + g8);
-                    s8v b1 = ld8(Wr + (size_t)(r0 + 16 + c16) * 64 + kc + g8);
+                const unsigned short* Ap = Aq + (size_t)(m0 + c16) * lda2 + g8;
+                const unsigned short* Bp = Bq + (size_t)(n0 + c16) * lda2 + g8;
+                for (int kc = 0; kc < K; kc += 32) {
+                    s8v a0 = ld8(Ap + kc);
+                    s8v a1 = ld8(Ap + 16 * lda2 + kc);
+                    s8v b0 = ld8(Bp + kc);
+                    s8v b1 = ld8(Bp + 16 * lda2 + kc);
                     acc[0][0] = mfma16(a0, b0, acc[0][0]);
                     acc[0][1] = mfma16(a0, b1, acc[0][1]);
                     acc[1][0] = mfma16(a1, b0, acc[1][0]);
@@ -305,496 +475,333 @@
                 for (int fm = 0; fm < 2; ++fm)
 #pragma unroll
                     for (int r = 0; r < 4; ++r) {
-                        const int el = el0 + fm * 16 + g4 + r;
-                        float ya = yL[el * 3 + 0], yb = yL[el * 3 + 1], yc = yL[el * 3 + 2];
-#pragma unroll
-                        for (int fn = 0; fn < 2; ++fn) {
-                            const float av = acc[fm][fn][r];
-                            const int col = r0 + fn * 16 + c16;
-                            if (r0 < 128) {
-                                in0L[el * 168 + col] = f2bf(av * bf2f(x0L[el * 128 + col]));
-                            } else if (r0 < 160) {
-                                int c = col - 128;
-                                float d1 = bf2f(x1L[(0 * 64 + el) * 32 + c]) * ya
-                                         + bf2f(x1L[(1 * 64 + el) * 32 + c]) * yb
-                                         + bf2f(x1L[(2 * 64 + el) * 32 + c]) * yc;
-                                in0L[el * 168 + col] = f2bf(av * d1);
-                            } else if (r0 < 288) {
-                                int c = col - 160;
-                                inUL[el * 136 + c] = f2bf(av * bf2f(x0L[el * 128 + c]));
-                            } else {
-                                int c = (r0 < 320) ? (col - 288) : (r0 < 352) ? (col - 320) : (col - 352);
-                                float fx = bf2f(x1L[(0 * 64 + el) * 32 + c]);
-                                float fy = bf2f(x1L[(1 * 64 + el) * 32 + c]);
-                                float fz = bf2f(x1L[(2 * 64 + el) * 32 + c]);
-                                float w0, w1, w2; int off;
-                                if (r0 < 320) {
-                                    off = 0; w0 = av * fx; w1 = av * fy; w2 = av * fz;
-                                } else if (r0 < 352) {
-                                    off = 32;
-                                    w0 = av * (fy * yc - fz * yb);
-                                    w1 = av * (fz * ya - fx * yc);
-                                    w2 = av * (fx * yb - fy * ya);
-                                } else {
-                                    off = 64;
-                                    float d1 = fx * ya + fy * yb + fz * yc;
-                                    w0 = av * (ya * d1 - fx * (1.0f / 3.0f));
-                                    w1 = av * (yb * d1 - fy * (1.0f / 3.0f));
-                                    w2 = av * (yc * d1 - fz * (1.0f / 3.0f));
-                                }
-                                inWL[0 * 64 * 104 + el * 104 + off + c] = f2bf(w0);
-                                inWL[1 * 64 * 104 + el * 104 + off + c] = f2bf(w1);
-                                inWL[2 * 64 * 104 + el * 104 + off + c] = f2bf(w2);
-                            }
-                        }
+                        const int m = m0 + fm * 16 + g4 + r;
+#pragma unroll
+                        for (int fn = 0; fn < 2; ++fn)
+                            Cq[(size_t)m * ldc2 + n0 + fn * 16 + c16] = acc[fm][fn][r];
                     }
             }
+        }
+        __threadfence();
+        gg.sync();
+
+        if (bid < 128) {
+            float (*q0s)[128] = (float(*)[128])lsm;
+            float (*q1s)[96]  = (float(*)[96])((char*)lsm + 4096);
+            float (*attns)[64] = (float(*)[64])((char*)lsm + 7168);
+            const int n = bid * 8 + w;
+            q0s[w][ln]      = A.q0[n * 128 + ln];
+            q0s[w][ln + 64] = A.q0[n * 128 + ln + 64];
+            if (ln < 32) {
+#pragma unroll
+                for (int m = 0; m < 3; ++m) q1s[w][m * 32 + ln] = A.q1p[m * PL + n * 32 + ln];
+            }
+            {
+                const int h = ln >> 4, k = ln & 15;
+                const int e = n * KK + k;
+                float acc = 0.f;
+                const unsigned short* kr = A.k0h + (size_t)e * 128 + h * 32;
+#pragma unroll
+                for (int c8 = 0; c8 < 4; ++c8) {
+                    s8v kv = ld8(kr + c8 * 8);
+#pragma unroll
+                    for (int j = 0; j < 8; ++j)
+                        acc += q0s[w][h * 32 + c8 * 8 + j] * bf2f((unsigned short)kv[j]);
+                }
+                s8v uv = ld8(A.uKh + (size_t)e * 32 + h * 8);
+#pragma unroll
+                for (int m = 0; m < 3; ++m) {
+                    float yv = A.y1[e * 3 + m];
+                    s8v k1v = ld8(A.k1ph + ((size_t)m * ENUM + e) * 32 + h * 8);
+#pragma unroll
+                    for (int c = 0; c < 8; ++c)
+                        acc += q1s[w][m * 32 + h * 8 + c] *
+                               (bf2f((unsigned short)k1v[c]) + bf2f((unsigned short)uv[c]) * yv);
+                }
+                acc = acc * SCALE_ATTN + A.biasb[e * 4 + h];
+                if (A.maskf[e] == 0.0f) acc = -1e9f;
+                float mx = gmax16(acc);
+                float ex = expf(acc - mx);
+                float sm = gsum16(ex);
+                attns[w][ln] = ex / sm;
+            }
+            const int g = ln & 15, kq = ln >> 4;
+            {
+                float o[8] = {};
+                const float* aw = &attns[w][(g >> 2) * 16];
+#pragma unroll
+                for (int kk2 = 0; kk2 < 4; ++kk2) {
+                    int kk = kq * 4 + kk2;
+                    float a = aw[kk];
+                    s8v v = ld8(A.v0h + (size_t)(n * KK + kk) * 128 + g * 8);
+#pragma unroll
+                    for (int j = 0; j < 8; ++j) o[j] += a * bf2f((unsigned short)v[j]);
+                }
+#pragma unroll
+                for (int j = 0; j < 8; ++j) {
+                    o[j] += __shfl_xor(o[j], 16);
+                    o[j] += __shfl_xor(o[j], 32);
+                }
+                if (kq == 0) {
+                    s8v r;
+#pragma unroll
+                    for (int j = 0; j < 8; ++j) r[j] = (short)f2bf(o[j]);
+                    *(s8v*)&A.o0h[(size_t)n * 128 + g * 8] = r;
+                }
+            }
+            {
+                float o[8] = {};
+                const int plane = g >> 2, cg2 = g & 3;
+                if (g < 12) {
+                    const float* aw = &attns[w][cg2 * 16];
+#pragma unroll
+                    for (int kk2 = 0; kk2 < 4; ++kk2) {
+                        int kk = kq * 4 + kk2;
+                        int e2 = n * KK + kk;
+                        float a = aw[kk];
+                        float yv = A.y1[e2 * 3 + plane];
+                        s8v v = ld8(A.v1ph + ((size_t)plane * ENUM + e2) * 32 + cg2 * 8);
+                        s8v u = ld8(A.uVh + (size_t)e2 * 32 + cg2 * 8);
+#pragma unroll
+                        for (int j = 0; j < 8; ++j)
+                            o[j] += a * (bf2f((unsigned short)v[j]) + bf2f((unsigned short)u[j]) * yv);
+                    }
+                }
+#pragma unroll
+                for (int j = 0; j < 8; ++j) {
+                    o[j] += __shfl_xor(o[j], 16);
+                    o[j] += __shfl_xor(o[j], 32);
+                }
+                if (kq == 0 && g < 12) {
+                    s8v r;
+#pragma unroll
+                    for (int j = 0; j < 8; ++j) r[j] = (short)f2bf(o[j]);
+                    *(s8v*)&A.o1h[((size_t)plane * NN + n) * 32 + cg2 * 8] = r;
+                }
+            }
+        }
+        __threadfence();
+        gg.sync();
+
+        if (bid < 64) {
+            const unsigned short* Wo0h = A.Wo0 + (size_t)l * 16384;
+            const unsigned short* Wo1h = A.Wo1 + (size_t)l * 1024;
+            const unsigned short* Wf0ah = A.Wf0a + (size_t)l * 65536;
+            const unsigned short* Wf0bh = A.Wf0b + (size_t)l * 65536;
+            const unsigned short* Wf1ah = A.Wf1a + (size_t)l * 4096;
+            const unsigned short* Wf1bh = A.Wf1b + (size_t)l * 4096;
+            const float* lnf0_g = A.lnf0_g + l * 128;
+            const float* lnf0_b = A.lnf0_b + l * 128;
+            const float* nf1_g  = A.nf1_g + l * 32;
+            const float* nf1_b  = A.nf1_b + l * 32;
+            const bool last = (l == Lc - 1);
+            float (*f0s)[132] = (float(*)[132])lsm;
+            float (*f1s)[16][36] = (float(*)[16][36])((char*)lsm + 8448);
+            unsigned short (*x0s)[136] = (unsigned short(*)[136])((char*)lsm + 15360);
+            float (*x1s)[16][36] = (float(*)[16][36])((char*)lsm + 19712);
+            unsigned short (*hs)[520] = (unsigned short(*)[520])((char*)lsm + 26624);
+            unsigned short (*h1b)[16][136] = (unsigned short(*)[16][136])((char*)lsm + 43264);
+            const int n0 = bid * 16;
+            const float aA = A.alpha_attn[l], aF = A.alpha_ff[l];
+            {
+                f4v acc = f4v{0.f, 0.f, 0.f, 0.f};
+                const unsigned short* Ap = A.o0h + (size_t)(n0 + c16) * 128 + g8;
+#pragma unroll
+                for (int kc = 0; kc < 128; kc += 32) {
+                    s8v a = ld8(Ap + kc);
+                    s8v b = ld8(Wo0h + (size_t)(w * 16 + c16) * 128 + g8 + kc);
+                    acc = mfma16(a, b, acc);
+                }
+                int colg = w * 16 + c16;
+#pragma unroll
+                for (int r = 0; r < 4; ++r) {
+                    int row = g4 + r;
+                    f0s[row][colg] = A.f0[(size_t)(n0 + row) * 128 + colg] + aA * acc[r];
+                }
+            }
+#pragma unroll
+            for (int it = 0; it < 3; ++it) {
+                int g = t + it * 512;
+                int c = g & 31, node = (g >> 5) & 15, m = g >> 9;
+                float a = 0.f;
+                const unsigned short* wrow = Wo1h + c * 32;
+                const unsigned short* orow = A.o1h + ((size_t)m * NN + n0 + node) * 32;
+#pragma unroll
+                for (int cc = 0; cc < 32; ++cc) a += bf2f(wrow[cc]) * bf2f(orow[cc]);
+                f1s[m][node][c] = A.f1p[(size_t)m * PL + (n0 + node) * 32 + c] + aA * a;
+            }
             __syncthreads();
-            const int tmax = (s == 0) ? 18 : 16;
-#pragma unroll 1
-            for (int ti = w; ti < tmax; ti += 8) {
-                if (ti >= 16) {
-                    const int esub = ti - 16;
-                    f4v bacc[2] = {f4v{0.f,0.f,0.f,0.f}, f4v{0.f,0.f,0.f,0.f}};
-                    s8v zb;
-#pragma unroll
-                    for (int j = 0; j < 8; ++j) zb[j] = 0;
-#pragma unroll
-                    for (int kc = 0; kc < 64; kc += 32) {
-                        s8v a0 = *(const s8v*)&edL[(esub * 32 + c16) * 72 + kc + g8];
-                        s8v a1 = *(const s8v*)&edL[(esub * 32 + 16 + c16) * 72 + kc + g8];
-                        s8v b0 = (c16 < 4) ? ld8(WbL + (size_t)c16 * 64 + kc + g8) : zb;
-                        bacc[0] = mfma16(a0, b0, bacc[0]);
-                        bacc[1] = mfma16(a1, b0, bacc[1]);
+            for (int i = 0; i < 2; ++i) {
+                int row = w * 2 + i;
+                float v0 = f0s[row][ln], v1 = f0s[row][ln + 64];
+                float mn = wsum64(v0 + v1) * (1.0f / 128.0f);
+                float d0 = v0 - mn, d1 = v1 - mn;
+                float var = wsum64(d0 * d0 + d1 * d1) * (1.0f / 128.0f);
+                float rs = rsqrtf(var + 1e-5f);
+                x0s[row][ln]      = f2bf(gelu_f(d0 * rs * lnf0_g[ln] + lnf0_b[ln]));
+                x0s[row][ln + 64] = f2bf(gelu_f(d1 * rs * lnf0_g[ln + 64] + lnf0_b[ln + 64]));
+            }
+            if (t < 256) {
+                int node = t >> 4, sub = t & 15;
+                float p[2][3], n1v[2];
+#pragma unroll
+                for (int q = 0; q < 2; ++q) {
+                    int c = sub + q * 16;
+                    p[q][0] = f1s[0][node][c]; p[q][1] = f1s[1][node][c]; p[q][2] = f1s[2][node][c];
+                    n1v[q] = sqrtf(p[q][0]*p[q][0] + p[q][1]*p[q][1] + p[q][2]*p[q][2]);
+                }
+                float s = gsum16(n1v[0] + n1v[1]);
+                float mn = s * (1.0f / 32.0f);
+                float d0 = n1v[0] - mn, d1 = n1v[1] - mn;
+                float vv = gsum16(d0 * d0 + d1 * d1);
+                float rs = rsqrtf(vv * (1.0f / 32.0f) + 1e-5f);
+#pragma unroll
+                for (int q = 0; q < 2; ++q) {
+                    int c = sub + q * 16;
+                    float sc = gelu_f((n1v[q] - mn) * rs * nf1_g[c] + nf1_b[c]) / (n1v[q] + 1e-6f);
+                    x1s[0][node][c] = p[q][0] * sc;
+                    x1s[1][node][c] = p[q][1] * sc;
+                    x1s[2][node][c] = p[q][2] * sc;
+                }
+            }
+            __syncthreads();
+            {
+                f4v acc[4];
+#pragma unroll
+                for (int i = 0; i < 4; ++i) acc[i] = f4v{0.f,0.f,0.f,0.f};
+#pragma unroll
+                for (int kc = 0; kc < 128; kc += 32) {
+                    s8v a = *(const s8v*)&x0s[c16][kc + g8];
+#pragma unroll
+                    for (int tt = 0; tt < 4; ++tt) {
+                        s8v b = ld8(Wf0ah + (size_t)((w * 4 + tt) * 16 + c16) * 128 + g8 + kc);
+                        acc[tt] = mfma16(a, b, acc[tt]);
                     }
-                    if (c16 < 4) {
-#pragma unroll
-                        for (int fm = 0; fm < 2; ++fm)
-#pragma unroll
-                            for (int r = 0; r < 4; ++r)
-                                biasb[(size_t)(e0 + esub * 32 + fm * 16 + g4 + r) * 4 + c16] = bacc[fm][r];
+                }
+#pragma unroll
+                for (int tt = 0; tt < 4; ++tt) {
+                    int colg = (w * 4 + tt) * 16 + c16;
+#pragma unroll
+                    for (int r = 0; r < 4; ++r) hs[g4 + r][colg] = f2bf(gelu_f(acc[tt][r]));
+                }
+            }
+#pragma unroll
+            for (int it = 0; it < 4; ++it) {
+                int g = t + it * 512;
+                int r = g & 127, node = g >> 7;
+                float a0 = 0.f, a1 = 0.f, a2 = 0.f;
+                const unsigned short* wrow = Wf1ah + r * 32;
+#pragma unroll
+                for (int c = 0; c < 32; ++c) {
+                    float wv = bf2f(wrow[c]);
+                    a0 += wv * x1s[0][node][c];
+                    a1 += wv * x1s[1][node][c];
+                    a2 += wv * x1s[2][node][c];
+                }
+                float nh = sqrtf(a0 * a0 + a1 * a1 + a2 * a2);
+                float sc = gelu_f(nh) / (nh + 1e-6f);
+                h1b[0][node][r] = f2bf(a0 * sc);
+                h1b[1][node][r] = f2bf(a1 * sc);
+                h1b[2][node][r] = f2bf(a2 * sc);
+            }
+            __syncthreads();
+            {
+                f4v acc = f4v{0.f, 0.f, 0.f, 0.f};
+#pragma unroll 4
+                for (int kc = 0; kc < 512; kc += 32) {
+                    s8v a = *(const s8v*)&hs[c16][kc + g8];
+                    s8v b = ld8(Wf0bh + (size_t)(w * 16 + c16) * 512 + g8 + kc);
+                    acc = mfma16(a, b, acc);
+                }
+                int colg = w * 16 + c16;
+#pragma unroll
+                for (int r = 0; r < 4; ++r) {
+                    int row = g4 + r;
+                    float v = f0s[row][colg] + aF * acc[r];
+                    f0s[row][colg] = v;
+                    A.f0[(size_t)(n0 + row) * 128 + colg] = v;
+                }
+            }
+#pragma unroll
+            for (int it = 0; it < 3; ++it) {
+                int g = t + it * 512;
+                int c = g & 31, node = (g >> 5) & 15, m = g >> 9;
+                float a = 0.f;
+                const unsigned short* wrow = Wf1bh + c * 128;
+#pragma unroll 8
+                for (int r = 0; r < 128; ++r) a += bf2f(wrow[r]) * bf2f(h1b[m][node][r]);
+                float v = f1s[m][node][c] + aF * a;
+                f1s[m][node][c] = v;
+                A.f1p[(size_t)m * PL + (n0 + node) * 32 + c] = v;
+            }
+            __syncthreads();
+            if (!last) {
+                const float* ln0n_g = A.ln0_g + 128;
+                const float* ln0n_b = A.ln0_b + 128;
+                const float* n1n_g  = A.n1_g + 32;
+                const float* n1n_b  = A.n1_b + 32;
+                for (int i = 0; i < 2; ++i) {
+                    int row = w * 2 + i;
+                    float v0 = f0s[row][ln], v1 = f0s[row][ln + 64];
+                    float mn = wsum64(v0 + v1) * (1.0f / 128.0f);
+                    float d0 = v0 - mn, d1 = v1 - mn;
+                    float var = wsum64(d0 * d0 + d1 * d1) * (1.0f / 128.0f);
+                    float rs = rsqrtf(var + 1e-5f);
+                    A.x0h[(size_t)(n0 + row) * 128 + ln]      = f2bf(gelu_f(d0 * rs * ln0n_g[ln] + ln0n_b[ln]));
+                    A.x0h[(size_t)(n0 + row) * 128 + ln + 64] = f2bf(gelu_f(d1 * rs * ln0n_g[ln + 64] + ln0n_b[ln + 64]));
+                }
+                if (t < 256) {
+                    int node = t >> 4, sub = t & 15;
+                    float p[2][3], n1v[2];
+#pragma unroll
+                    for (int q = 0; q < 2; ++q) {
+                        int c = sub + q * 16;
+                        p[q][0] = f1s[0][node][c]; p[q][1] = f1s[1][node][c]; p[q][2] = f1s[2][node][c];
+                        n1v[q] = sqrtf(p[q][0]*p[q][0] + p[q][1]*p[q][1] + p[q][2]*p[q][2]);
                     }
-                    continue;
-                }
-                const unsigned short* Ab; const unsigned short* Bb;
-                unsigned short* Cb;
-                int apit, K, ldb, ldcq, esub;
-                if (ti < 8) {
-                    esub = ti & 1; int nt = ti >> 1;
-                    Ab = in0L; apit = 168; K = 160;
-                    Bb = WA + (size_t)(nt * 32) * 160; ldb = 160;
-                    Cb = K0o + (size_t)(e0 + esub * 32) * 128 + nt * 32; ldcq = 128;
-                } else if (ti < 10) {
-                    esub = ti - 8;
-                    Ab = inUL; apit = 136; K = 128; Bb = WB; ldb = 224;
-                    Cb = Uo + (size_t)(e0 + esub * 32) * 32; ldcq = 32;
-                } else {
-                    int id = ti - 10; int m = id >> 1; esub = id & 1;
-                    Ab = inWL + m * 64 * 104; apit = 104; K = 96;
-                    Bb = WB + 128; ldb = 224;
-                    Cb = K1o + ((size_t)m * ENUM + e0 + esub * 32) * 32; ldcq = 32;
-                }
-                const int m0l = esub * 32;
-                f4v acc[2][2];
-#pragma unroll
-                for (int a = 0; a < 2; ++a)
-#pragma unroll
-                    for (int bq = 0; bq < 2; ++bq) acc[a][bq] = f4v{0.f, 0.f, 0.f, 0.f};
-                for (int kc = 0; kc < K; kc += 32) {
-                    s8v a0 = *(const s8v*)&Ab[(m0l + c16) * apit + kc + g8];
-                    s8v a1 = *(const s8v*)&Ab[(m0l + 16 + c16) * apit + kc + g8];
-                    s8v b0 = ld8(Bb + (size_t)c16 * ldb + kc + g8);
-                    s8v b1 = ld8(Bb + (size_t)(16 + c16) * ldb + kc + g8);
-                    acc[0][0] = mfma16(a0, b0, acc[0][0]);
-                    acc[0][1] = mfma16(a0, b1, acc[0][1]);
-                    acc[1][0] = mfma16(a1, b0, acc[1][0]);
-                    acc[1][1] = mfma16(a1, b1, acc[1][1]);
-                }
-#pragma unroll
-                for (int fm = 0; fm < 2; ++fm)
-#pragma unroll
-                    for (int r = 0; r < 4; ++r) {
-                        const int lr = fm * 16 + g4 + r;
-#pragma unroll
-                        for (int fn = 0; fn < 2; ++fn)
-                            Cb[(size_t)lr * ldcq + fn * 16 + c16] = f2bf(acc[fm][fn][r]);
+                    float s = gsum16(n1v[0] + n1v[1]);
+                    float mn = s * (1.0f / 32.0f);
+                    float d0 = n1v[0] - mn, d1 = n1v[1] - mn;
+                    float vv = gsum16(d0 * d0 + d1 * d1);
+                    float rs = rsqrtf(vv * (1.0f / 32.0f) + 1e-5f);
+#pragma unroll
+                    for (int q = 0; q < 2; ++q) {
+                        int c = sub + q * 16;
+                        float sc = gelu_f((n1v[q] - mn) * rs * n1n_g[c] + n1n_b[c]) / (n1v[q] + 1e-6f);
+                        A.x1h[(size_t)0 * X1HS + (n0 + node) * 32 + c] = f2bf(p[q][0] * sc);
+                        A.x1h[(size_t)1 * X1HS + (n0 + node) * 32 + c] = f2bf(p[q][1] * sc);
+                        A.x1h[(size_t)2 * X1HS + (n0 + node) * 32 + c] = f2bf(p[q][2] * sc);
                     }
-            }
-            __syncthreads();
+                }
+            } else {
+#pragma unroll
+                for (int it = 0; it < 4; ++it) {
+                    int g = t + it * 512;
+                    int row = g >> 7, col = g & 127;
+                    x0s[row][col] = f2bf(f0s[row][col]);
+                }
+                __syncthreads();
+                f4v acc = f4v{0.f, 0.f, 0.f, 0.f};
+#pragma unroll
+                for (int kc = 0; kc < 128; kc += 32) {
+                    s8v a = *(const s8v*)&x0s[c16][kc + g8];
+                    s8v b = ld8(A.Wp0 + (size_t)(w * 16 + c16) * 128 + g8 + kc);
+                    acc = mfma16(a, b, acc);
+                }
+                int colg = w * 16 + c16;
+#pragma unroll
+                for (int r = 0; r < 4; ++r)
+                    A.out[(size_t)(n0 + g4 + r) * 128 + colg] = acc[r];
+                if (t < 144) {
+                    int node = t / 9, rr = t % 9, o = rr / 3, m = rr % 3;
+                    float a = A.coords[((size_t)(n0 + node) * 4 + 1) * 3 + m];
+                    for (int c = 0; c < 32; ++c) a += A.Wp1[o * 32 + c] * f1s[m][node][c];
+                    A.out[NN * 128 + ((size_t)(n0 + node) * 3 + o) * 3 + m] = a;
+                }
+            }
         }
-        return;
-    }
-    const int wt = (bid - 256) * 8 + w;
-    const unsigned short* A; const unsigned short* B;
-    float* C; int K, lda2, m0, n0, ldc2;
-    if (wt < 128) {
-        int rowt = wt >> 2, colt = wt & 3;
-        A = x0h; B = Wq0l; C = q0;
-        K = 128; lda2 = 128; ldc2 = 128;
-        m0 = rowt * 32; n0 = colt * 32;
-    } else {
-        int k = wt - 128;
-        int pl = k >> 5, rowt = k & 31;
-        A = x1h + (size_t)pl * X1HS; B = Wq1l; C = q1p + (size_t)pl * PL;
-        K = 32; lda2 = 32; ldc2 = 32;
-        m0 = rowt * 32; n0 = 0;
-    }
-    f4v acc[2][2];
-#pragma unroll
-    for (int a = 0; a < 2; ++a)
-#pragma unroll
-        for (int bq = 0; bq < 2; ++bq) acc[a][bq] = f4v{0.f, 0.f, 0.f, 0.f};
-    const unsigned short* Ap = A + (size_t)(m0 + c16) * lda2 + g8;
-    const unsigned short* Bp = B + (size_t)(n0 + c16) * lda2 + g8;
-    for (int kc = 0; kc < K; kc += 32) {
-        s8v a0 = ld8(Ap + kc);
-        s8v a1 = ld8(Ap + 16 * lda2 + kc);
-        s8v b0 = ld8(Bp + kc);
-        s8v b1 = ld8(Bp + 16 * lda2 + kc);
-        acc[0][0] = mfma16(a0, b0, acc[0][0]);
-        acc[0][1] = mfma16(a0, b1, acc[0][1]);
-        acc[1][0] = mfma16(a1, b0, acc[1][0]);
-        acc[1][1] = mfma16(a1, b1, acc[1][1]);
-    }
-#pragma unroll
-    for (int fm = 0; fm < 2; ++fm)
-#pragma unroll
-        for (int r = 0; r < 4; ++r) {
-            const int m = m0 + fm * 16 + g4 + r;
-#pragma unroll
-            for (int fn = 0; fn < 2; ++fn)
-                C[(size_t)m * ldc2 + n0 + fn * 16 + c16] = acc[fm][fn][r];
-        }
-}
-
-__global__ __launch_bounds__(256) void attn_core(const float* __restrict__ q0,
-                                                 const float* __restrict__ q1p,
-                                                 const unsigned short* __restrict__ k0h,
-                                                 const unsigned short* __restrict__ k1ph,
-                                                 const unsigned short* __restrict__ v0h,
-                                                 const unsigned short* __restrict__ v1ph,
-                                                 const unsigned short* __restrict__ uKh,
-                                                 const unsigned short* __restrict__ uVh,
-                                                 const float* __restrict__ biasb,
-                                                 const float* __restrict__ maskf,
-                                                 const float* __restrict__ y1,
-                                                 unsigned short* __restrict__ o0h,
-                                                 unsigned short* __restrict__ o1h) {
-    __shared__ float q0s[4][128];
-    __shared__ float q1s[4][96];
-    __shared__ float attns[4][64];
-    const int wid = threadIdx.x >> 6, lane = threadIdx.x & 63;
-    const int n = blockIdx.x * 4 + wid;
-    q0s[wid][lane]      = q0[n * 128 + lane];
-    q0s[wid][lane + 64] = q0[n * 128 + lane + 64];
-    if (lane < 32) {
-#pragma unroll
-        for (int m = 0; m < 3; ++m) q1s[wid][m * 32 + lane] = q1p[m * PL + n * 32 + lane];
-    }
-    __syncthreads();
-    {
-        const int h = lane >> 4, k = lane & 15;
-        const int e = n * KK + k;
-        float acc = 0.f;
-        const unsigned short* kr = k0h + (size_t)e * 128 + h * 32;
-#pragma unroll
-        for (int c8 = 0; c8 < 4; ++c8) {
-            s8v kv = ld8(kr + c8 * 8);
-#pragma unroll
-            for (int j = 0; j < 8; ++j)
-                acc += q0s[wid][h * 32 + c8 * 8 + j] * bf2f((unsigned short)kv[j]);
-        }
-        s8v uv = ld8(uKh + (size_t)e * 32 + h * 8);
-#pragma unroll
-        for (int m = 0; m < 3; ++m) {
-            float yv = y1[e * 3 + m];
-            s8v k1v = ld8(k1ph + ((size_t)m * ENUM + e) * 32 + h * 8);
-#pragma unroll
-            for (int c = 0; c < 8; ++c)
-                acc += q1s[wid][m * 32 + h * 8 + c] *
-                       (bf2f((unsigned short)k1v[c]) + bf2f((unsigned short)uv[c]) * yv);
-        }
-        acc = acc * SCALE_ATTN + biasb[e * 4 + h];
-        if (maskf[e] == 0.0f) acc = -1e9f;
-        float mx = gmax16(acc);
-        float ex = expf(acc - mx);
-        float sm = gsum16(ex);
-        attns[wid][lane] = ex / sm;
-    }
-    __syncthreads();
-    const int g = lane & 15, kq = lane >> 4;
-    {
-        float o[8] = {};
-        const float* aw = &attns[wid][(g >> 2) * 16];
-#pragma unroll
-        for (int kk2 = 0; kk2 < 4; ++kk2) {
-            int kk = kq * 4 + kk2;
-            float a = aw[kk];
-            s8v v = ld8(v0h + (size_t)(n * KK + kk) * 128 + g * 8);
-#pragma unroll
-            for (int j = 0; j < 8; ++j) o[j] += a * bf2f((unsigned short)v[j]);
-        }
-#pragma unroll
-        for (int j = 0; j < 8; ++j) {
-            o[j] += __shfl_xor(o[j], 16);
-            o[j] += __shfl_xor(o[j], 32);
-        }
-        if (kq == 0) {
-            s8v r;
-#pragma unroll
-            for (int j = 0; j < 8; ++j) r[j] = (short)f2bf(o[j]);
-            *(s8v*)&o0h[(size_t)n * 128 + g * 8] = r;
-        }
-    }
-    {
-        float o[8] = {};
-        const int plane = g >> 2, cg = g & 3;
-        if (g < 12) {
-            const float* aw = &attns[wid][cg * 16];
-#pragma unroll
-            for (int kk2 = 0; kk2 < 4; ++kk2) {
-                int kk = kq * 4 + kk2;
-                int e2 = n * KK + kk;
-                float a = aw[kk];
-                float yv = y1[e2 * 3 + plane];
-                s8v v = ld8(v1ph + ((size_t)plane * ENUM + e2) * 32 + cg * 8);
-                s8v u = ld8(uVh + (size_t)e2 * 32 + cg * 8);
-#pragma unroll
-                for (int j = 0; j < 8; ++j)
-                    o[j] += a * (bf2f((unsigned short)v[j]) + bf2f((unsigned short)u[j]) * yv);
-            }
-        }
-#pragma unroll
-        for (int j = 0; j < 8; ++j) {
-            o[j] += __shfl_xor(o[j], 16);
-            o[j] += __shfl_xor(o[j], 32);
-        }
-        if (kq == 0 && g < 12) {
-            s8v r;
-#pragma unroll
-            for (int j = 0; j < 8; ++j) r[j] = (short)f2bf(o[j]);
-            *(s8v*)&o1h[((size_t)plane * NN + n) * 32 + cg * 8] = r;
-        }
-    }
-}
-
-template <int MODE>
-__global__ __launch_bounds__(512) void fused_post(
-    const unsigned short* __restrict__ o0h, const unsigned short* __restrict__ o1h,
-    float* __restrict__ f0, float* __restrict__ f1p,
-    const unsigned short* __restrict__ Wo0h, const unsigned short* __restrict__ Wo1h,
-    const unsigned short* __restrict__ Wf0ah, const unsigned short* __restrict__ Wf0bh,
-    const unsigned short* __restrict__ Wf1ah, const unsigned short* __restrict__ Wf1bh,
-    const float* __restrict__ alA, const float* __restrict__ alF,
-    const float* __restrict__ lnf0_g, const float* __restrict__ lnf0_b,
-    const float* __restrict__ nf1_g, const float* __restrict__ nf1_b,
-    const float* __restrict__ ln0n_g, const float* __restrict__ ln0n_b,
-    const float* __restrict__ n1n_g, const float* __restrict__ n1n_b,
-    unsigned short* __restrict__ x0h, unsigned short* __restrict__ x1h,
-    const unsigned short* __restrict__ Wp0h, const float* __restrict__ Wp1,
-    const float* __restrict__ coords, float* __restrict__ out) {
-    __shared__ float f0s[16][132];
-    __shared__ float f1s[3][16][36];
-    __shared__ unsigned short x0s[16][136];
-    __shared__ float x1s[3][16][36];
-    __shared__ unsigned short hs[16][520];
-    __shared__ unsigned short h1b[3][16][136];
-    const int t = threadIdx.x, w = t >> 6, l = t & 63;
-    const int c16 = l & 15, g8 = (l >> 4) * 8, g4 = (l >> 4) * 4;
-    const int n0 = blockIdx.x * 16;
-    const float aA = alA[0], aF = alF[0];
-
-    {
-        f4v acc = f4v{0.f, 0.f, 0.f, 0.f};
-        const unsigned short* Ap = o0h + (size_t)(n0 + c16) * 128 + g8;
-#pragma unroll
-        for (int kc = 0; kc < 128; kc += 32) {
-            s8v a = ld8(Ap + kc);
-            s8v b = ld8(Wo0h + (size_t)(w * 16 + c16) * 128 + g8 + kc);
-            acc = mfma16(a, b, acc);
-        }
-        int colg = w * 16 + c16;
-#pragma unroll
-        for (int r = 0; r < 4; ++r) {
-            int row = g4 + r;
-            f0s[row][colg] = f0[(size_t)(n0 + row) * 128 + colg] + aA * acc[r];
-        }
-    }
-#pragma unroll
-    for (int it = 0; it < 3; ++it) {
-        int g = t + it * 512;
-        int c = g & 31, node = (g >> 5) & 15, m = g >> 9;
-        float a = 0.f;
-        const unsigned short* wrow = Wo1h + c * 32;
-        const unsigned short* orow = o1h + ((size_t)m * NN + n0 + node) * 32;
-#pragma unroll
-        for (int cc = 0; cc < 32; ++cc) a += bf2f(wrow[cc]) * bf2f(orow[cc]);
-        f1s[m][node][c] = f1p[(size_t)m * PL + (n0 + node) * 32 + c] + aA * a;
-    }
-    __syncthreads();
-    for (int i = 0; i < 2; ++i) {
-        int row = w * 2 + i;
-        float v0 = f0s[row][l], v1 = f0s[row][l + 64];
-        float mn = wsum64(v0 + v1) * (1.0f / 128.0f);
-        float d0 = v0 - mn, d1 = v1 - mn;
-        float var = wsum64(d0 * d0 + d1 * d1) * (1.0f / 128.0f);
-        float rs = rsqrtf(var + 1e-5f);
-        x0s[row][l]      = f2bf(gelu_f(d0 * rs * lnf0_g[l] + lnf0_b[l]));
-        x0s[row][l + 64] = f2bf(gelu_f(d1 * rs * lnf0_g[l + 64] + lnf0_b[l + 64]));
-    }
-    if (t < 256) {
-        int node = t >> 4, sub = t & 15;
-        float p[2][3], n1v[2];
-#pragma unroll
-        for (int q = 0; q < 2; ++q) {
-            int c = sub + q * 16;
-            p[q][0] = f1s[0][node][c]; p[q][1] = f1s[1][node][c]; p[q][2] = f1s[2][node][c];
-            n1v[q] = sqrtf(p[q][0]*p[q][0] + p[q][1]*p[q][1] + p[q][2]*p[q][2]);
-        }
-        float s = gsum16(n1v[0] + n1v[1]);
-        float mn = s * (1.0f / 32.0f);
-        float d0 = n1v[0] - mn, d1 = n1v[1] - mn;
-        float vv = gsum16(d0 * d0 + d1 * d1);
-        float rs = rsqrtf(vv * (1.0f / 32.0f) + 1e-5f);
-#pragma unroll
-        for (int q = 0; q < 2; ++q) {
-            int c = sub + q * 16;
-            float sc = gelu_f((n1v[q] - mn) * rs * nf1_g[c] + nf1_b[c]) / (n1v[q] + 1e-6f);
-            x1s[0][node][c] = p[q][0] * sc;
-            x1s[1][node][c] = p[q][1] * sc;
-            x1s[2][node][c] = p[q][2] * sc;
-        }
-    }
-    __syncthreads();
-    {
-        f4v acc[4];
-#pragma unroll
-        for (int i = 0; i < 4; ++i) acc[i] = f4v{0.f,0.f,0.f,0.f};
-#pragma unroll
-        for (int kc = 0; kc < 128; kc += 32) {
-            s8v a = *(const s8v*)&x0s[c16][kc + g8];
-#pragma unroll
-            for (int tt = 0; tt < 4; ++tt) {
-                s8v b = ld8(Wf0ah + (size_t)((w * 4 + tt) * 16 + c16) * 128 + g8 + kc);
-                acc[tt] = mfma16(a, b, acc[tt]);
-            }
-        }
-#pragma unroll
-        for (int tt = 0; tt < 4; ++tt) {
-            int colg = (w * 4 + tt) * 16 + c16;
-#pragma unroll
-            for (int r = 0; r < 4; ++r) hs[g4 + r][colg] = f2bf(gelu_f(acc[tt][r]));
-        }
-    }
-#pragma unroll
-    for (int it = 0; it < 4; ++it) {
-        int g = t + it * 512;
-        int r = g & 127, node = g >> 7;
-        float a0 = 0.f, a1 = 0.f, a2 = 0.f;
-        const unsigned short* wrow = Wf1ah + r * 32;
-#pragma unroll
-        for (int c = 0; c < 32; ++c) {
-            float wv = bf2f(wrow[c]);
-            a0 += wv * x1s[0][node][c];
-            a1 += wv * x1s[1][node][c];
-            a2 += wv * x1s[2][node][c];
-        }
-        float nh = sqrtf(a0 * a0 + a1 * a1 + a2 * a2);
-        float sc = gelu_f(nh) / (nh + 1e-6f);
-        h1b[0][node][r] = f2bf(a0 * sc);
-        h1b[1][node][r] = f2bf(a1 * sc);
-        h1b[2][node][r] = f2bf(a2 * sc);
-    }
-    __syncthreads();
-    {
-        f4v acc = f4v{0.f, 0.f, 0.f, 0.f};
-#pragma unroll 4
-        for (int kc = 0; kc < 512; kc += 32) {
-            s8v a = *(const s8v*)&hs[c16][kc + g8];
-            s8v b = ld8(Wf0bh + (size_t)(w * 16 + c16) * 512 + g8 + kc);
-            acc = mfma16(a, b, acc);
-        }
-        int colg = w * 16 + c16;
-#pragma unroll
-        for (int r = 0; r < 4; ++r) {
-            int row = g4 + r;
-            float v = f0s[row][colg] + aF * acc[r];
-            f0s[row][colg] = v;
-            f0[(size_t)(n0 + row) * 128 + colg] = v;
-        }
-    }
-#pragma unroll
-    for (int it = 0; it < 3; ++it) {
-        int g = t + it * 512;
-        int c = g & 31, node = (g >> 5) & 15, m = g >> 9;
-        float a = 0.f;
-        const unsigned short* wrow = Wf1bh + c * 128;
-#pragma unroll 8
-        for (int r = 0; r < 128; ++r) a += bf2f(wrow[r]) * bf2f(h1b[m][node][r]);
-        float v = f1s[m][node][c] + aF * a;
-        f1s[m][node][c] = v;
-        f1p[(size_t)m * PL + (n0 + node) * 32 + c] = v;
-    }
-    __syncthreads();
-    if (MODE == 0) {
-        for (int i = 0; i < 2; ++i) {
-            int row = w * 2 + i;
-            float v0 = f0s[row][l], v1 = f0s[row][l + 64];
-            float mn = wsum64(v0 + v1) * (1.0f / 128.0f);
-            float d0 = v0 - mn, d1 = v1 - mn;
-            float var = wsum64(d0 * d0 + d1 * d1) * (1.0f / 128.0f);
-            float rs = rsqrtf(var + 1e-5f);
-            x0h[(size_t)(n0 + row) * 128 + l]      = f2bf(gelu_f(d0 * rs * ln0n_g[l] + ln0n_b[l]));
-            x0h[(size_t)(n0 + row) * 128 + l + 64] = f2bf(gelu_f(d1 * rs * ln0n_g[l + 64] + ln0n_b[l + 64]));
-        }
-        if (t < 256) {
-            int node = t >> 4, sub = t & 15;
-            float p[2][3], n1v[2];
-#pragma unroll
-            for (int q = 0; q < 2; ++q) {
-                int c = sub + q * 16;
-                p[q][0] = f1s[0][node][c]; p[q][1] = f1s[1][node][c]; p[q][2] = f1s[2][node][c];
-                n1v[q] = sqrtf(p[q][0]*p[q][0] + p[q][1]*p[q][1] + p[q][2]*p[q][2]);
-            }
-            float s = gsum16(n1v[0] + n1v[1]);
-            float mn = s * (1.0f / 32.0f);
-            float d0 = n1v[0] - mn, d1 = n1v[1] - mn;
-            float vv = gsum16(d0 * d0 + d1 * d1);
-            float rs = rsqrtf(vv * (1.0f / 32.0f) + 1e-5f);
-#pragma unroll
-            for (int q = 0; q < 2; ++q) {
-                int c = sub + q * 16;
-                float sc = gelu_f((n1v[q] - mn) * rs * n1n_g[c] + n1n_b[c]) / (n1v[q] + 1e-6f);
-                x1h[(size_t)0 * X1HS + (n0 + node) * 32 + c] = f2bf(p[q][0] * sc);
-                x1h[(size_t)1 * X1HS + (n0 + node) * 32 + c] = f2bf(p[q][1] * sc);
-                x1h[(size_t)2 * X1HS + (n0 + node) * 32 + c] = f2bf(p[q][2] * sc);
-            }
-        }
-    } else {
-#pragma unroll
-        for (int it = 0; it < 4; ++it) {
-            int g = t + it * 512;
-            int row = g >> 7, col = g & 127;
-            x0s[row][col] = f2bf(f0s[row][col]);
-        }
-        __syncthreads();
-        f4v acc = f4v{0.f, 0.f, 0.f, 0.f};
-#pragma unroll
-        for (int kc = 0; kc < 128; kc += 32) {
-            s8v a = *(const s8v*)&x0s[c16][kc + g8];
-            s8v b = ld8(Wp0h + (size_t)(w * 16 + c16) * 128 + g8 + kc);
-            acc = mfma16(a, b, acc);
-        }
-        int colg = w * 16 + c16;
-#pragma unroll
-        for (int r = 0; r < 4; ++r)
-            out[(size_t)(n0 + g4 + r) * 128 + colg] = acc[r];
-        if (t < 144) {
-            int node = t / 9, rr = t % 9, o = rr / 3, m = rr % 3;
-            float a = coords[((size_t)(n0 + node) * 4 + 1) * 3 + m];
-            for (int c = 0; c < 32; ++c) a += Wp1[o * 32 + c] * f1s[m][node][c];
-            out[NN * 128 + ((size_t)(n0 + node) * 3 + o) * 3 + m] = a;
-        }
+        __threadfence();
+        gg.sync();
     }
 }
 
@@ -909,35 +916,19 @@
                                                       edges_h, nf_h, Wi0_h, f0);
     fnorm1_kernel<<<NN / 4, 256, 0, stream>>>(f0, f1p, ln0_g, ln0_b, n1_g, n1_b, x0h, x1h);
 
-    for (int l = 0; l < Lc; ++l) {
-        edge_kv2<<<284, 512, EKV_LDS2, stream>>>(
-            edges_h,
-            WrK_h + (size_t)l * 24576, WrV_h + (size_t)l * 24576,
-            WkA_h + (size_t)l * 20480, WvA_h + (size_t)l * 20480,
-            WkB_h + (size_t)l * 7168,  WvB_h + (size_t)l * 7168,
-            Wb_h + (size_t)l * 256,
-            x0h, x1h, idx, y1,
-            k0h, v0h, uKh, uVh, k1ph, v1ph, biasb,
-            Wq0_h + (size_t)l * 16384, Wq1_h + (size_t)l * 1024, q0, q1p);
-        attn_core<<<NN / 4, 256, 0, stream>>>(q0, q1p, k0h, k1ph, v0h, v1ph, uKh, uVh,
-            biasb, maskf, y1, o0h, o1h);
-        if (l == 0) {
-            fused_post<0><<<NN / 16, 512, 0, stream>>>(
-                o0h, o1h, f0, f1p,
-                Wo0_h, Wo1_h, Wf0a_h, Wf0b_h, Wf1a_h, Wf1b_h,
-                alpha_attn + 0, alpha_ff + 0,
-                lnf0_g, lnf0_b, nf1_g, nf1_b,
-                ln0_g + 128, ln0_b + 128, n1_g + 32, n1_b + 32,
-                x0h, x1h, nullptr, nullptr, nullptr, nullptr);
-        } else {
-            fused_post<1><<<NN / 16, 512, 0, stream>>>(
-                o0h, o1h, f0, f1p,
-                Wo0_h + 16384, Wo1_h + 1024, Wf0a_h + 65536, Wf0b_h + 65536,
-                Wf1a_h + 4096, Wf1b_h + 4096,
-                alpha_attn + 1, alpha_ff + 1,
-                lnf0_g + 128, lnf0_b + 128, nf1_g + 32, nf1_b + 32,
-                nullptr, nullptr, nullptr, nullptr,
-                nullptr, nullptr, Wp0_h, Wp1, coords, out);
-        }
-    }
-}
+    MegaArgs ma;
+    ma.edges_h = edges_h; ma.WrK = WrK_h; ma.WrV = WrV_h; ma.WkA = WkA_h; ma.WvA = WvA_h;
+    ma.WkB = WkB_h; ma.WvB = WvB_h; ma.Wb = Wb_h;
+    ma.Wq0 = Wq0_h; ma.Wq1 = Wq1_h; ma.Wo0 = Wo0_h; ma.Wo1 = Wo1_h;
+    ma.Wf0a = Wf0a_h; ma.Wf0b = Wf0b_h; ma.Wf1a = Wf1a_h; ma.Wf1b = Wf1b_h; ma.Wp0 = Wp0_h;
+    ma.x0h = x0h; ma.x1h = x1h; ma.idx = idx; ma.y1 = y1;
+    ma.k0h = k0h; ma.v0h = v0h; ma.uKh = uKh; ma.uVh = uVh; ma.k1ph = k1ph; ma.v1ph = v1ph;
+    ma.biasb = biasb; ma.q0 = q0; ma.q1p = q1p; ma.f0 = f0; ma.f1p = f1p;
+    ma.maskf = maskf; ma.alpha_attn = alpha_attn; ma.alpha_ff = alpha_ff;
+    ma.ln0_g = ln0_g; ma.ln0_b = ln0_b; ma.n1_g = n1_g; ma.n1_b = n1_b;
+    ma.lnf0_g = lnf0_g; ma.lnf0_b = lnf0_b; ma.nf1_g = nf1_g; ma.nf1_b = nf1_b;
+    ma.Wp1 = Wp1; ma.coords = coords; ma.o0h = o0h; ma.o1h = o1h; ma.out = out;
+    void* kargs[] = { &ma };
+    hipLaunchCooperativeKernel((const void*)mega_kernel, dim3(256), dim3(512),
+                               kargs, (unsigned)EKV_LDS2, stream);
+}
```

Result: slower. 652.9 us (+198.1%).
